# Kernel optimization log

Hardware: AMD Instinct MI355X
Metric: run time of the kernel (lower is better)

## Reference

```python
import jax, jax.numpy as jnp
import numpy as np

NQ, NT, NRF, K, M, B = 8, 16, 4, 4, 2, 28
N_OUTER, N_INNER = 120, 20

def _ry(t):
    c, s = jnp.cos(t / 2), jnp.sin(t / 2)
    return jnp.stack([jnp.stack([c, -s]), jnp.stack([s, c])]).astype(jnp.complex64)

def _rz(t):
    e = jnp.exp(-0.5j * t)
    z = jnp.zeros_like(e)
    return jnp.stack([jnp.stack([e, z]), jnp.stack([z, jnp.conj(e)])])

def _rot(phi, theta, omega):  # pennylane Rot = RZ(omega) RY(theta) RZ(phi)
    return _rz(omega) @ _ry(theta) @ _rz(phi)

def _ap1(state, U, w):
    return jnp.moveaxis(jnp.tensordot(U, state, axes=[[1], [w]]), 0, w)

def _cnot(state, c, t):
    s = jnp.moveaxis(state, (c, t), (0, 1))
    s = s.at[1].set(s[1, ::-1])
    return jnp.moveaxis(s, (0, 1), (c, t))

def _qcircuit(inp, w):  # inp [2*NQ] angles, w [3,NQ,3] -> [NQ] PauliZ expvals
    st = jnp.zeros((2,) * NQ, jnp.complex64).at[(0,) * NQ].set(1.0)
    for i in range(NQ):
        st = _ap1(st, _ry(inp[i]), i)
        st = _ap1(st, _rz(inp[i + NQ]), i)
    for l in range(3):
        for i in range(NQ):
            st = _ap1(st, _rot(w[l, i, 0], w[l, i, 1], w[l, i, 2]), i)
        for i in range(NQ - 1):
            st = _cnot(st, i, i + 1)
        st = _cnot(st, NQ - 1, 0)
    p = jnp.abs(st) ** 2
    z = [jnp.moveaxis(p, i, 0)[0].sum() - jnp.moveaxis(p, i, 0)[1].sum() for i in range(NQ)]
    return jnp.stack(z).astype(jnp.float32)

def _qblock(x, p):  # x [B,80] -> [B,out]
    W1, b1, W2, b2, W3, b3, qw, Wp, bp = p
    h = jnp.tanh(x @ W1.T + b1)
    h = jnp.tanh(h @ W2.T + b2)
    ang = h @ W3.T + b3  # [B, 2*NQ]
    q = jax.vmap(_qcircuit, in_axes=(0, None))(ang, qw)  # [B, NQ]
    return q @ Wp.T + bp

def _to_complex(x):
    return x[..., 0::2] + 1j * x[..., 1::2]

def _sum_rate(H, F, W, Pt):
    Heff = jnp.einsum('kbmn,nbr,kbru->kbmu', H, F[0], W)  # [K,B,M,M]
    G = jnp.einsum('kbmu,kbvu->kbmv', Heff, jnp.conj(Heff))
    A = jnp.eye(M, dtype=G.dtype) + Pt * G
    return jnp.sum(jnp.log2(jnp.abs(jnp.linalg.det(A).real) + 1e-12), axis=0).astype(jnp.float32)

def _beam_err(H, F, W, R, Pt):
    X = jnp.einsum('nbr,kbru->kbnu', F[0], W)  # [K,B,NT,M]
    C = jnp.einsum('kbnu,kbvu->kbnv', X, jnp.conj(X))  # [K,B,NT,NT]
    return jnp.mean(jnp.sqrt(jnp.sum(jnp.abs(C - R) ** 2, axis=(2, 3)) + 1e-12), axis=0).astype(jnp.float32)

def _normalize(F, W, H, Pt):
    F = F / (jnp.abs(F) + 1e-12)
    X = jnp.einsum('nbr,kbru->kbnu', F[0], W)
    pw = jnp.sum(jnp.abs(X) ** 2, axis=(0, 2, 3))  # [B]
    return F, W * jnp.sqrt(Pt / (pw + 1e-12))[None, :, None, None]

def _initialize(H, R, Pt, key):
    k1, k2 = jax.random.split(key)
    ph = jax.random.uniform(k1, (1, NT, B, NRF), maxval=2 * np.pi)
    F = jnp.exp(1j * ph).astype(jnp.complex64)
    W = jax.random.normal(k2, (K, B, NRF, M), dtype=jnp.complex64)
    return _normalize(F, W, H, Pt)

def _state(H, F, W, R, Wproj, bproj):
    s = jnp.concatenate([
        jnp.abs(F).mean((0, 1)).reshape(-1),    # B*NRF
        jnp.angle(F).mean((0, 1)).reshape(-1),  # B*NRF
        jnp.abs(W).mean((0, 1, 2)),             # M
        jnp.angle(W).mean((0, 1, 2)),           # M
        jnp.abs(H).mean((0, 1, 2)).reshape(-1), # NT
        jnp.abs(R).mean((0, 1)).reshape(-1),    # NT*NT  -> total 500
    ])
    return jnp.broadcast_to(s @ Wproj.T + bproj, (B, Wproj.shape[0]))

def _forward(H, R, Pt, step, qFp, qWp, Wproj, bproj):
    F, W = _initialize(H, R, Pt, jax.random.key(1))
    r0, t0 = _sum_rate(H, F, W, Pt), _beam_err(H, F, W, R, Pt)
    base = jax.random.key(7)

    def outer(carry, it):
        F, W = carry
        k = jax.random.fold_in(base, it)
        st = _state(H, F, W, R, Wproj, bproj)  # [B,80]

        def inner(c, p):
            Fc, kk = c
            kk, kn = jax.random.split(kk)
            dF = _to_complex(_qblock(st, p)).reshape(B, NT, NRF).transpose(1, 0, 2)[None]
            noise = jax.random.normal(kn, Fc.shape, dtype=jnp.complex64)
            Fc = Fc + step * noise * 0.001 + dF * 0.001
            return (Fc / (jnp.abs(Fc) + 1e-12), kk), None

        (F, k), _ = jax.lax.scan(inner, (F, k), qFp)
        dW = _to_complex(_qblock(st, qWp)).reshape(B, K, NRF, M).transpose(1, 0, 2, 3)
        k, kn = jax.random.split(k)
        W = W + step * jax.random.normal(kn, W.shape, dtype=jnp.complex64) * 0.001 + dW * 0.001
        F, W = _normalize(F, W, H, Pt)
        return (F, W), (_sum_rate(H, F, W, Pt), _beam_err(H, F, W, R, Pt))

    (F, W), (rs, ts) = jax.lax.scan(outer, (F, W), jnp.arange(N_OUTER))
    rates = jnp.concatenate([r0[None], rs], axis=0).T  # [B, N_OUTER+1]
    taus = jnp.concatenate([t0[None], ts], axis=0).T
    return rates, taus, F, W


def setup_inputs() -> dict:
    key = jax.random.key(0)
    ks = jax.random.split(key, 32)
    r = lambda i, sh: jax.random.normal(ks[i], sh, dtype=jnp.float32)
    WS = 0.1  # weight init scale for tanh stability
    return {
        'H_re': r(0, (K, B, M, NT)), 'H_im': r(1, (K, B, M, NT)),
        'R_re': r(2, (K, B, NT, NT)), 'R_im': r(3, (K, B, NT, NT)),
        'Pt': jnp.ones((1,), jnp.float32),
        'step': jnp.ones((1,), jnp.float32) * 0.02,
        'qF_W1': r(4, (N_INNER, 64, 80)) * WS, 'qF_b1': r(5, (N_INNER, 64)) * WS,
        'qF_W2': r(6, (N_INNER, 32, 64)) * WS, 'qF_b2': r(7, (N_INNER, 32)) * WS,
        'qF_W3': r(8, (N_INNER, 16, 32)) * WS, 'qF_b3': r(9, (N_INNER, 16)) * WS,
        'qF_qw': r(10, (N_INNER, 3, NQ, 3)), 'qF_Wp': r(11, (N_INNER, 128, NQ)) * WS,
        'qF_bp': r(12, (N_INNER, 128)) * WS,
        'qW_W1': r(13, (64, 80)) * WS, 'qW_b1': r(14, (64,)) * WS,
        'qW_W2': r(15, (32, 64)) * WS, 'qW_b2': r(16, (32,)) * WS,
        'qW_W3': r(17, (16, 32)) * WS, 'qW_b3': r(18, (16,)) * WS,
        'qW_qw': r(19, (3, NQ, 3)), 'qW_Wp': r(20, (64, NQ)) * WS,
        'qW_bp': r(21, (64,)) * WS,
        'proj_W': r(22, (80, 500)) * WS, 'proj_b': r(23, (80,)) * WS,
    }


def reference(H_re, H_im, R_re, R_im, Pt, step, qF_W1, qF_b1, qF_W2, qF_b2, qF_W3, qF_b3,
              qF_qw, qF_Wp, qF_bp, qW_W1, qW_b1, qW_W2, qW_b2, qW_W3, qW_b3, qW_qw, qW_Wp,
              qW_bp, proj_W, proj_b):
    H = (H_re + 1j * H_im).astype(jnp.complex64)
    R = (R_re + 1j * R_im).astype(jnp.complex64)
    qFp = (qF_W1, qF_b1, qF_W2, qF_b2, qF_W3, qF_b3, qF_qw, qF_Wp, qF_bp)
    qWp = (qW_W1, qW_b1, qW_W2, qW_b2, qW_W3, qW_b3, qW_qw, qW_Wp, qW_bp)
    return _forward(H, R, Pt[0], step[0], qFp, qWp, proj_W, proj_b)
```

## Files before the change

### kernel.cpp

```cpp
#include <hip/hip_runtime.h>
#include <stdint.h>

#define NT_   16
#define NRF_  4
#define K_    4
#define M_    2
#define B_    28
#define NOUT_ 120
#define NIN_  20
#define FN_   1792
#define WN_   896
#define XN_   3584
#define TJOB_ 8704
#define TSZ_  (21*TJOB_)
#define O_TAUS 3388
#define O_F    6776
#define O_W    10360

typedef float2 cf;
__device__ __forceinline__ cf cmul(cf a, cf b){ return make_float2(a.x*b.x - a.y*b.y, a.x*b.y + a.y*b.x); }
__device__ __forceinline__ cf cmulc(cf a, cf b){ return make_float2(a.x*b.x + a.y*b.y, a.y*b.x - a.x*b.y); }
__device__ __forceinline__ cf cadd(cf a, cf b){ return make_float2(a.x + b.x, a.y + b.y); }
__device__ __forceinline__ cf csc(float s, cf a){ return make_float2(s*a.x, s*a.y); }
__device__ __forceinline__ cf shflc(cf v, int m){ return make_float2(__shfl_xor(v.x, m, 64), __shfl_xor(v.y, m, 64)); }

__device__ __forceinline__ uint32_t rotl32(uint32_t x, int r){ return (x << r) | (x >> (32 - r)); }

__device__ __forceinline__ void threefry(uint32_t k0, uint32_t k1, uint32_t x0, uint32_t x1,
                                         uint32_t &o0, uint32_t &o1){
  uint32_t ks2 = k0 ^ k1 ^ 0x1BD11BDAu;
  x0 += k0; x1 += k1;
#define TF4(a,b,c,d) \
  x0 += x1; x1 = rotl32(x1,(a)); x1 ^= x0; \
  x0 += x1; x1 = rotl32(x1,(b)); x1 ^= x0; \
  x0 += x1; x1 = rotl32(x1,(c)); x1 ^= x0; \
  x0 += x1; x1 = rotl32(x1,(d)); x1 ^= x0;
  TF4(13,15,26,6)  x0 += k1;  x1 += ks2 + 1u;
  TF4(17,29,16,24) x0 += ks2; x1 += k0 + 2u;
  TF4(13,15,26,6)  x0 += k0;  x1 += k1 + 3u;
  TF4(17,29,16,24) x0 += k1;  x1 += ks2 + 4u;
  TF4(13,15,26,6)  x0 += ks2; x1 += k0 + 5u;
#undef TF4
  o0 = x0; o1 = x1;
}

__device__ __forceinline__ void ksplit(uint2 k, uint2 &ka, uint2 &kb){
  threefry(k.x, k.y, 0u, 0u, ka.x, ka.y);
  threefry(k.x, k.y, 0u, 1u, kb.x, kb.y);
}
__device__ __forceinline__ uint2 kfold(uint2 k, uint32_t d){
  uint2 r; threefry(k.x, k.y, 0u, d, r.x, r.y); return r;
}
__device__ __forceinline__ uint32_t rbits(uint2 k, uint32_t i){
  uint32_t a, b; threefry(k.x, k.y, 0u, i, a, b); return a ^ b;
}

__device__ __forceinline__ float bits_to_unit(uint32_t b){
  return __uint_as_float((b >> 9) | 0x3f800000u) - 1.0f;
}

__device__ __forceinline__ float erfinv_f32(float x){
  float w = -log1pf(-x * x);
  float p;
  if (w < 5.0f){
    w = w - 2.5f;
    p =  2.81022636e-08f;
    p = fmaf(p, w,  3.43273939e-07f);
    p = fmaf(p, w, -3.5233877e-06f);
    p = fmaf(p, w, -4.39150654e-06f);
    p = fmaf(p, w,  0.00021858087f);
    p = fmaf(p, w, -0.00125372503f);
    p = fmaf(p, w, -0.00417768164f);
    p = fmaf(p, w,  0.246640727f);
    p = fmaf(p, w,  1.50140941f);
  } else {
    w = sqrtf(w) - 3.0f;
    p = -0.000200214257f;
    p = fmaf(p, w,  0.000100950558f);
    p = fmaf(p, w,  0.00134934322f);
    p = fmaf(p, w, -0.00367342844f);
    p = fmaf(p, w,  0.00573950773f);
    p = fmaf(p, w, -0.0076224613f);
    p = fmaf(p, w,  0.00943887047f);
    p = fmaf(p, w,  1.00167406f);
    p = fmaf(p, w,  2.83297682f);
  }
  return p * x;
}

#define SQRT2F 1.41421356f

__device__ __forceinline__ float normal_from_bits(uint32_t b){
  const float lo = -0.99999994f;
  float u = bits_to_unit(b);
  float v = fmaxf(lo, u * 2.0f + lo);
  return SQRT2F * erfinv_f32(v);
}

__device__ __forceinline__ cf cnormal(uint2 kre, uint2 kim, uint32_t e){
  float re = normal_from_bits(rbits(kre, e));
  float im = normal_from_bits(rbits(kim, e));
  return make_float2(re / SQRT2F, im / SQRT2F);
}

__device__ void noise_key_chain(uint32_t it, uint2 *out){
  uint2 k = kfold(make_uint2(0u, 7u), it);
  for (int j = 0; j < NIN_; ++j){
    uint2 kk, kn;
    ksplit(k, kk, kn);
    k = kk;
    ksplit(kn, out[2*j], out[2*j + 1]);
  }
  uint2 k2, knW;
  ksplit(k, k2, knW);
  ksplit(knW, out[40], out[41]);
}

#define QELEM_ ((NIN_*FN_)/4)
__global__ __launch_bounds__(1024)
void rng_kernel(float2* __restrict__ wsF, float2* __restrict__ wsW,
                float2* __restrict__ wsIW,
                float* __restrict__ wsT, float* __restrict__ wsU,
                float* __restrict__ wsC, float2* __restrict__ wsFst,
                float2* __restrict__ wsWst,
                const float* __restrict__ H_re, const float* __restrict__ H_im,
                const float* __restrict__ R_re, const float* __restrict__ R_im,
                const float* __restrict__ qF_qw, const float* __restrict__ qW_qw,
                const float* __restrict__ qF_W1, const float* __restrict__ qF_W2,
                const float* __restrict__ qF_W3, const float* __restrict__ qF_Wp,
                const float* __restrict__ qW_W1, const float* __restrict__ qW_W2,
                const float* __restrict__ qW_W3, const float* __restrict__ qW_Wp){
  __shared__ uint2 keys[42];
  const int bi = blockIdx.x, t = threadIdx.x;
  if (bi < 4*NOUT_){
    const int it = bi >> 2, q = bi & 3;
    if (t == 0) noise_key_chain((uint32_t)it, keys);
    __syncthreads();
    const int base = q*QELEM_;
    for (int idx = base + t; idx < base + QELEM_; idx += 1024){
      int j = idx / FN_, e = idx - j*FN_;
      wsF[(size_t)it*(NIN_*FN_) + idx] = cnormal(keys[2*j], keys[2*j + 1], (uint32_t)e);
    }
    if (q == 0){
      for (int e = t; e < WN_; e += 1024)
        wsW[(size_t)it*WN_ + e] = cnormal(keys[40], keys[41], (uint32_t)e);
    }
  } else if (bi == 4*NOUT_){
    if (t == 0){
      uint2 k1, k2;
      ksplit(make_uint2(0u, 1u), k1, k2);
      keys[0] = k1;
      ksplit(k2, keys[1], keys[2]);
    }
    __syncthreads();
    const float TWOPI = 6.28318530717958647692f;
    for (int e = t; e < FN_; e += 1024){
      float u = bits_to_unit(rbits(keys[0], (uint32_t)e));
      float ph = fmaxf(0.0f, u * TWOPI);
      float s, c; sincosf(ph, &s, &c);
      wsFst[e] = make_float2(c, s);
    }
    for (int e = t; e < WN_; e += 1024){
      cf w = cnormal(keys[1], keys[2], (uint32_t)e);
      wsIW[e] = w;
      wsWst[e] = w;
    }
  } else if (bi < 4*NOUT_ + 1 + 21){
    const int j = bi - (4*NOUT_ + 1);
    const bool isW = (j == 20);
    const float* W1 = isW ? qW_W1 : qF_W1 + j*(64*80);
    const float* W2 = isW ? qW_W2 : qF_W2 + j*(32*64);
    const float* W3 = isW ? qW_W3 : qF_W3 + j*(16*32);
    const float* Wp = isW ? qW_Wp : qF_Wp + j*(128*8);
    float* dst = wsT + j*TJOB_;
    for (int idx = t; idx < 5120; idx += 1024){
      int q = idx >> 6, i = idx & 63;
      dst[idx] = W1[i*80 + q];
    }
    for (int idx = t; idx < 2048; idx += 1024){
      int q = idx >> 5, i = idx & 31;
      dst[5120 + idx] = W2[i*64 + q];
    }
    for (int idx = t; idx < 512; idx += 1024){
      int q = idx >> 4, i = idx & 15;
      dst[7168 + idx] = W3[i*32 + q];
    }
    const int nOut = isW ? 64 : 128;
    for (int idx = t; idx < 8*nOut; idx += 1024){
      int z = idx / nOut, o = idx - z*nOut;
      dst[7680 + z*128 + o] = Wp[o*8 + z];
    }
  } else {
    if (t < 504){
      int j = t / 24, gg = t - j*24;
      const float* qw = (j == 20) ? qW_qw : qF_qw + j*72;
      float phi = qw[gg*3], th = qw[gg*3 + 1], om = qw[gg*3 + 2];
      float sh, ch; sincosf(0.5f*th, &sh, &ch);
      float sp, cp; sincosf(0.5f*(phi + om), &sp, &cp);
      float sm, cm; sincosf(0.5f*(phi - om), &sm, &cm);
      float* u = wsU + t*8;
      u[0] =  ch*cp; u[1] = -ch*sp;
      u[2] = -sh*cm; u[3] = -sh*sm;
      u[4] =  sh*cm; u[5] = -sh*sm;
      u[6] =  ch*cp; u[7] =  ch*sp;
    } else if (t < 520){
      int n = t - 504;
      float s = 0.f;
      for (int kbm = 0; kbm < 224; ++kbm){
        float re = H_re[kbm*16 + n], im = H_im[kbm*16 + n];
        s += sqrtf(re*re + im*im);
      }
      wsC[n] = s * (1.0f/224.0f);
    } else if (t < 776){
      int nv = t - 520;
      float s = 0.f;
      for (int kb = 0; kb < 112; ++kb){
        float re = R_re[kb*256 + nv], im = R_im[kb*256 + nv];
        s += sqrtf(re*re + im*im);
      }
      wsC[16 + nv] = s * (1.0f/112.0f);
    }
  }
}

__device__ __forceinline__ void gate(int q, cf u00, cf u01, cf u10, cf u11,
                                     cf &a0, cf &a1, cf &a2, cf &a3, int lane){
  if (q == 7){
    cf n0 = cadd(cmul(u00, a0), cmul(u01, a1));
    cf n1 = cadd(cmul(u10, a0), cmul(u11, a1));
    cf n2 = cadd(cmul(u00, a2), cmul(u01, a3));
    cf n3 = cadd(cmul(u10, a2), cmul(u11, a3));
    a0 = n0; a1 = n1; a2 = n2; a3 = n3;
  } else if (q == 6){
    cf n0 = cadd(cmul(u00, a0), cmul(u01, a2));
    cf n2 = cadd(cmul(u10, a0), cmul(u11, a2));
    cf n1 = cadd(cmul(u00, a1), cmul(u01, a3));
    cf n3 = cadd(cmul(u10, a1), cmul(u11, a3));
    a0 = n0; a1 = n1; a2 = n2; a3 = n3;
  } else {
    const int m = 1 << (5 - q);
    const bool hi = (lane & m) != 0;
    cf cO = hi ? u11 : u00;
    cf cP = hi ? u10 : u01;
    cf p0 = shflc(a0, m), p1 = shflc(a1, m), p2 = shflc(a2, m), p3 = shflc(a3, m);
    a0 = cadd(cmul(cO, a0), cmul(cP, p0));
    a1 = cadd(cmul(cO, a1), cmul(cP, p1));
    a2 = cadd(cmul(cO, a2), cmul(cP, p2));
    a3 = cadd(cmul(cO, a3), cmul(cP, p3));
  }
}

__device__ void run_circuit2(const float* trig, const float* uni, int lane, float z[8]){
  cf a0 = make_float2(lane == 0 ? 1.f : 0.f, 0.f);
  cf a1 = make_float2(0.f, 0.f), a2 = make_float2(0.f, 0.f), a3 = make_float2(0.f, 0.f);
  #pragma unroll
  for (int i = 0; i < 8; ++i){
    float sh = trig[2*i],      ch = trig[2*i + 1];
    float sp = trig[16 + 2*i], cp = trig[16 + 2*i + 1];
    float sm = trig[32 + 2*i], cm = trig[32 + 2*i + 1];
    cf u00 = make_float2( ch*cp, -ch*sp);
    cf u11 = make_float2( ch*cp,  ch*sp);
    cf u01 = make_float2(-sh*cm, -sh*sm);
    cf u10 = make_float2( sh*cm, -sh*sm);
    gate(i, u00, u01, u10, u11, a0, a1, a2, a3, lane);
  }
  for (int l = 0; l < 3; ++l){
    #pragma unroll
    for (int i = 0; i < 8; ++i){
      const float* u = uni + (l*8 + i)*8;
      gate(i, make_float2(u[0], u[1]), make_float2(u[2], u[3]),
              make_float2(u[4], u[5]), make_float2(u[6], u[7]), a0, a1, a2, a3, lane);
    }
    #pragma unroll
    for (int i = 0; i < 5; ++i){
      const int cm_ = 1 << (5 - i), tm = 1 << (4 - i);
      const bool c = (lane & cm_) != 0;
      cf p0 = shflc(a0, tm), p1 = shflc(a1, tm), p2 = shflc(a2, tm), p3 = shflc(a3, tm);
      a0 = c ? p0 : a0; a1 = c ? p1 : a1; a2 = c ? p2 : a2; a3 = c ? p3 : a3;
    }
    {
      const bool c = (lane & 1) != 0;
      cf t0 = c ? a2 : a0, t2 = c ? a0 : a2;
      cf t1 = c ? a3 : a1, t3 = c ? a1 : a3;
      a0 = t0; a1 = t1; a2 = t2; a3 = t3;
    }
    { cf tmp = a2; a2 = a3; a3 = tmp; }
    a1 = shflc(a1, 32);
    a3 = shflc(a3, 32);
  }
  const float p0 = a0.x*a0.x + a0.y*a0.y;
  const float p1 = a1.x*a1.x + a1.y*a1.y;
  const float p2 = a2.x*a2.x + a2.y*a2.y;
  const float p3 = a3.x*a3.x + a3.y*a3.y;
  const float tot = p0 + p1 + p2 + p3;
  z[6] = (p0 + p1) - (p2 + p3);
  z[7] = (p0 + p2) - (p1 + p3);
  #pragma unroll
  for (int i = 0; i < 6; ++i)
    z[i] = ((lane >> (5 - i)) & 1) ? -tot : tot;
  #pragma unroll
  for (int m = 1; m < 64; m <<= 1){
    #pragma unroll
    for (int i = 0; i < 8; ++i) z[i] += __shfl_xor(z[i], m, 64);
  }
}

__global__ __launch_bounds__(640)
void k_qblock2(const float* __restrict__ wsT, const float* __restrict__ wsU,
               const float* __restrict__ wsC,
               const float* __restrict__ wsFeatA, const float* __restrict__ wsFeatG,
               const float* __restrict__ wsPart,
               const float* __restrict__ projW, const float* __restrict__ projB,
               const float* __restrict__ qF_b1, const float* __restrict__ qF_b2,
               const float* __restrict__ qF_b3, const float* __restrict__ qF_bp,
               const float* __restrict__ qW_b1, const float* __restrict__ qW_b2,
               const float* __restrict__ qW_b3, const float* __restrict__ qW_bp,
               float2* __restrict__ wsdF, float2* __restrict__ wsdW){
  const int j = blockIdx.x;
  const int t = threadIdx.x;
  const int lane = t & 63;
  const int wv = t >> 6;
  const bool isW = (j == 20);
  __shared__ float sS[500];
  __shared__ float sSt[80];
  __shared__ float mlp[160];
  __shared__ float luni[192];
  for (int i = t; i < 192; i += 640) luni[i] = wsU[j*192 + i];
  for (int i = t; i < 112; i += 640){ sS[i] = wsFeatA[i]; sS[112 + i] = wsFeatG[i]; }
  if (t < 4){
    float s = 0.f;
    for (int bb = 0; bb < 28; ++bb) s += wsPart[bb*4 + t];
    sS[224 + t] = s * (1.0f/448.0f);
  }
  for (int i = t; i < 272; i += 640) sS[228 + i] = wsC[i];
  __syncthreads();
  {
    int o = wv*8 + (lane >> 3), i = lane & 7;
    const float* row = projW + o*500;
    float acc = 0.f;
    #pragma unroll
    for (int s = 0; s < 63; ++s){
      int j2 = i + 8*s;
      if (j2 < 500) acc = fmaf(sS[j2], row[j2], acc);
    }
    #pragma unroll
    for (int m = 1; m < 8; m <<= 1) acc += __shfl_xor(acc, m, 64);
    if (i == 0) sSt[o] = acc + projB[o];
  }
  __syncthreads();

  if (t < 64){
    const float* b1 = isW ? qW_b1 : qF_b1 + j*64;
    const float* b2 = isW ? qW_b2 : qF_b2 + j*32;
    const float* b3 = isW ? qW_b3 : qF_b3 + j*16;
    const float* bp = isW ? qW_bp : qF_bp + j*128;
    const float* w1t = wsT + j*TJOB_;
    const float* w2t = w1t + 5120;
    const float* w3t = w1t + 7168;
    const float* wpt = w1t + 7680;

    {
      float acc = b1[lane];
      for (int q = 0; q < 80; ++q) acc = fmaf(w1t[q*64 + lane], sSt[q], acc);
      mlp[lane] = tanhf(acc);
    }
    __builtin_amdgcn_wave_barrier();
    {
      int i2 = lane & 31;
      float acc = b2[i2];
      for (int q = 0; q < 64; ++q) acc = fmaf(w2t[q*32 + i2], mlp[q], acc);
      float h2 = tanhf(acc);
      __builtin_amdgcn_wave_barrier();
      if (lane < 32) mlp[64 + lane] = h2;
    }
    __builtin_amdgcn_wave_barrier();
    {
      int i3 = lane & 15;
      float acc = b3[i3];
      for (int q = 0; q < 32; ++q) acc = fmaf(w3t[q*16 + i3], mlp[64 + q], acc);
      __builtin_amdgcn_wave_barrier();
      if (lane < 16) mlp[96 + lane] = acc;
    }
    __builtin_amdgcn_wave_barrier();
    if (lane < 24){
      int i = lane & 7, which = lane >> 3;
      float th = mlp[96 + i], om = mlp[96 + 8 + i];
      float arg = (which == 0) ? 0.5f*th
                : (which == 1) ? 0.5f*(0.f + om)
                               : 0.5f*(0.f - om);
      float s, c; sincosf(arg, &s, &c);
      mlp[112 + which*16 + 2*i]     = s;
      mlp[112 + which*16 + 2*i + 1] = c;
    }
    __builtin_amdgcn_wave_barrier();
    float z[8];
    run_circuit2(mlp + 112, luni, lane, z);
    if (!isW){
      float o0 = bp[lane];
      float o1 = bp[64 + lane];
      #pragma unroll
      for (int i = 0; i < 8; ++i){
        o0 = fmaf(wpt[i*128 + lane],      z[i], o0);
        o1 = fmaf(wpt[i*128 + 64 + lane], z[i], o1);
      }
      __builtin_amdgcn_wave_barrier();
      mlp[lane] = o0; mlp[64 + lane] = o1;
      __builtin_amdgcn_wave_barrier();
      wsdF[j*64 + lane] = make_float2(mlp[2*lane], mlp[2*lane + 1]);
    } else {
      float o0 = bp[lane];
      #pragma unroll
      for (int i = 0; i < 8; ++i) o0 = fmaf(wpt[i*128 + lane], z[i], o0);
      __builtin_amdgcn_wave_barrier();
      mlp[lane] = o0;
      __builtin_amdgcn_wave_barrier();
      if (lane < 32) wsdW[lane] = make_float2(mlp[2*lane], mlp[2*lane + 1]);
    }
  }
}

__global__ __launch_bounds__(128)
void k_update(const float* __restrict__ H_re, const float* __restrict__ H_im,
              const float* __restrict__ R_re, const float* __restrict__ R_im,
              const float* __restrict__ Pt_p, const float* __restrict__ step_p,
              const float2* __restrict__ wsF, const float2* __restrict__ wsW,
              const float2* __restrict__ wsdF, const float2* __restrict__ wsdW,
              float2* __restrict__ wsFst, float2* __restrict__ wsWst,
              float* __restrict__ wsFeatA, float* __restrict__ wsFeatG,
              float* __restrict__ wsPart,
              float* __restrict__ out, int it, int mode){
  const int b = blockIdx.x;
  const int t = threadIdx.x;
  __shared__ cf lF[64];
  __shared__ cf lW[32];
  __shared__ cf lX[128];
  __shared__ float scrA[96], scrG[96];
  __shared__ float red2[2];
  __shared__ float sscale;
  __shared__ float heR[16], heI[16];
  __shared__ float sKBl[4], sKB2l[4];
  const float c1 = step_p[0] * 0.001f;
  const float Ptv = Pt_p[0];

  if (t < 64){
    const int n = t >> 2, r = t & 3;
    const int e = n*112 + b*4 + r;
    cf F = wsFst[e];
    if (mode){
      const float2* np = wsF + (size_t)it*(NIN_*FN_);
      cf nzA[10], dvA[10], nzB[10], dvB[10];
      #pragma unroll
      for (int s = 0; s < 10; ++s){ nzA[s] = np[s*FN_ + e];        dvA[s] = wsdF[s*64 + t]; }
      #pragma unroll
      for (int s = 0; s < 10; ++s){ nzB[s] = np[(10 + s)*FN_ + e]; dvB[s] = wsdF[(10 + s)*64 + t]; }
      #pragma unroll
      for (int s = 0; s < 10; ++s){
        F.x = F.x + c1*nzA[s].x + 0.001f*dvA[s].x;
        F.y = F.y + c1*nzA[s].y + 0.001f*dvA[s].y;
        float rr = sqrtf(F.x*F.x + F.y*F.y) + 1e-12f;
        F.x /= rr; F.y /= rr;
      }
      #pragma unroll
      for (int s = 0; s < 10; ++s){
        F.x = F.x + c1*nzB[s].x + 0.001f*dvB[s].x;
        F.y = F.y + c1*nzB[s].y + 0.001f*dvB[s].y;
        float rr = sqrtf(F.x*F.x + F.y*F.y) + 1e-12f;
        F.x /= rr; F.y /= rr;
      }
    }
    float rr = sqrtf(F.x*F.x + F.y*F.y) + 1e-12f;
    F.x /= rr; F.y /= rr;
    lF[t] = F;
    wsFst[e] = F;
  } else if (t < 96){
    const int wi = t - 64;
    const int k = wi >> 3, ru = wi & 7;
    const int ew = (k*28 + b)*8 + ru;
    cf w = wsWst[ew];
    if (mode){
      cf nw = wsW[(size_t)it*WN_ + ew];
      cf dw = wsdW[k*8 + ru];
      w.x = w.x + c1*nw.x + 0.001f*dw.x;
      w.y = w.y + c1*nw.y + 0.001f*dw.y;
    }
    lW[wi] = w;
  }
  __syncthreads();
  {
    int u = t & 1, n = (t >> 1) & 15, k = t >> 5;
    const cf* fr = lF + n*4;
    const cf* wr = lW + k*8 + u;
    cf acc = cmul(fr[0], wr[0]);
    acc = cadd(acc, cmul(fr[1], wr[2]));
    acc = cadd(acc, cmul(fr[2], wr[4]));
    acc = cadd(acc, cmul(fr[3], wr[6]));
    lX[t] = acc;
  }
  __syncthreads();
  {
    float s = lX[t].x*lX[t].x + lX[t].y*lX[t].y;
    #pragma unroll
    for (int m = 1; m < 64; m <<= 1) s += __shfl_xor(s, m, 64);
    if ((t & 63) == 0) red2[t >> 6] = s;
  }
  __syncthreads();
  if (t == 0) sscale = sqrtf(Ptv / ((red2[0] + red2[1]) + 1e-12f));
  __syncthreads();
  const float sc = sscale;
  if (t < 32){
    const int k = t >> 3, ru = t & 7;
    const int ew = (k*28 + b)*8 + ru;
    cf w = csc(sc, lW[t]);
    lW[t] = w;
    wsWst[ew] = w;
  }
  lX[t] = csc(sc, lX[t]);
  __syncthreads();
  if (t < 16){
    const int k = t >> 2, ent = t & 3;
    const int m = ent >> 1, u = ent & 1;
    const float* hr = H_re + (k*28 + b)*32 + m*16;
    const float* hi = H_im + (k*28 + b)*32 + m*16;
    cf He = make_float2(0.f, 0.f);
    for (int n = 0; n < 16; ++n){
      cf h = make_float2(hr[n], hi[n]);
      He = cadd(He, cmul(h, lX[k*32 + n*2 + u]));
    }
    heR[t] = He.x; heI[t] = He.y;
  }
  __builtin_amdgcn_wave_barrier();
  if (t < 4){
    const int k = t;
    cf He00 = make_float2(heR[k*4 + 0], heI[k*4 + 0]);
    cf He01 = make_float2(heR[k*4 + 1], heI[k*4 + 1]);
    cf He10 = make_float2(heR[k*4 + 2], heI[k*4 + 2]);
    cf He11 = make_float2(heR[k*4 + 3], heI[k*4 + 3]);
    cf G00 = cadd(cmulc(He00, He00), cmulc(He01, He01));
    cf G01 = cadd(cmulc(He00, He10), cmulc(He01, He11));
    cf G10 = cadd(cmulc(He10, He00), cmulc(He11, He01));
    cf G11 = cadd(cmulc(He10, He10), cmulc(He11, He11));
    cf A00 = make_float2(1.f + Ptv*G00.x, Ptv*G00.y);
    cf A01 = csc(Ptv, G01);
    cf A10 = csc(Ptv, G10);
    cf A11 = make_float2(1.f + Ptv*G11.x, Ptv*G11.y);
    float detre = (A00.x*A11.x - A00.y*A11.y) - (A01.x*A10.x - A01.y*A10.y);
    sKBl[k] = log2f(fabsf(detre) + 1e-12f);
  }
  {
    const int k = t >> 5, i = t & 31;
    const float* rr = R_re + (k*28 + b)*256;
    const float* ri = R_im + (k*28 + b)*256;
    float acc = 0.f;
    #pragma unroll
    for (int c = 0; c < 8; ++c){
      int nv = c*32 + i;
      int n = nv >> 4, v = nv & 15;
      cf xn0 = lX[k*32 + n*2], xn1 = lX[k*32 + n*2 + 1];
      cf xv0 = lX[k*32 + v*2], xv1 = lX[k*32 + v*2 + 1];
      cf C = cadd(cmulc(xn0, xv0), cmulc(xn1, xv1));
      float dr = C.x - rr[nv], di = C.y - ri[nv];
      acc += dr*dr + di*di;
    }
    #pragma unroll
    for (int m = 1; m < 32; m <<= 1) acc += __shfl_xor(acc, m, 64);
    if (i == 0) sKB2l[k] = sqrtf(acc + 1e-12f);
  }
  __syncthreads();
  if (t == 0){
    const int slot = mode ? (it + 1) : 0;
    out[b*121 + slot] = sKBl[0] + sKBl[1] + sKBl[2] + sKBl[3];
    out[O_TAUS + b*121 + slot] = 0.25f*(sKB2l[0] + sKB2l[1] + sKB2l[2] + sKB2l[3]);
  }
  if (t < 64){
    cf f = lF[t];
    scrA[t] = sqrtf(f.x*f.x + f.y*f.y);
    scrG[t] = atan2f(f.y, f.x);
  } else if (t < 96){
    cf w = lW[t - 64];
    scrA[t] = sqrtf(w.x*w.x + w.y*w.y);
    scrG[t] = atan2f(w.y, w.x);
  }
  __syncthreads();
  if (t < 8){
    int r = t & 3;
    const float* src = (t < 4) ? scrA : scrG;
    float s = 0.f;
    for (int n = 0; n < 16; ++n) s += src[n*4 + r];
    float* dst = (t < 4) ? wsFeatA : wsFeatG;
    dst[b*4 + r] = s * (1.0f/16.0f);
  } else if (t >= 8 && t < 12){
    int tt = t - 8;
    int u = tt & 1; bool isG = tt >= 2;
    const float* src = isG ? scrG : scrA;
    float s = 0.f;
    for (int i = 0; i < 16; ++i) s += src[64 + i*2 + u];
    wsPart[b*4 + tt] = s;
  }
}

__global__ __launch_bounds__(1024)
void k_out(const float2* __restrict__ wsFst, const float2* __restrict__ wsWst,
           float* __restrict__ out, int fmode){
  const int t = threadIdx.x;
  if (fmode == 1){
    for (int e = t; e < FN_; e += 1024){
      out[O_F + e]       = wsFst[e].x;
      out[O_F + FN_ + e] = wsFst[e].y;
    }
    for (int e = t; e < WN_; e += 1024){
      out[O_W + e]       = wsWst[e].x;
      out[O_W + WN_ + e] = wsWst[e].y;
    }
  } else if (fmode == 2){
    for (int e = t; e < FN_; e += 1024) out[O_F + e] = wsFst[e].x;
    for (int e = t; e < WN_; e += 1024) out[O_F + FN_ + e] = wsWst[e].x;
  } else {
    for (int e = t; e < FN_; e += 1024){
      out[O_F + 2*e]     = wsFst[e].x;
      out[O_F + 2*e + 1] = wsFst[e].y;
    }
    for (int e = t; e < WN_; e += 1024){
      out[O_W + 2*e]     = wsWst[e].x;
      out[O_W + 2*e + 1] = wsWst[e].y;
    }
  }
}

__global__ __launch_bounds__(1024)
void main_kernel(const float* __restrict__ H_re, const float* __restrict__ H_im,
                 const float* __restrict__ R_re, const float* __restrict__ R_im,
                 const float* __restrict__ Pt_p, const float* __restrict__ step_p,
                 const float* __restrict__ qF_W1, const float* __restrict__ qF_b1,
                 const float* __restrict__ qF_W2, const float* __restrict__ qF_b2,
                 const float* __restrict__ qF_W3, const float* __restrict__ qF_b3,
                 const float* __restrict__ qF_qw, const float* __restrict__ qF_Wp,
                 const float* __restrict__ qF_bp,
                 const float* __restrict__ qW_W1, const float* __restrict__ qW_b1,
                 const float* __restrict__ qW_W2, const float* __restrict__ qW_b2,
                 const float* __restrict__ qW_W3, const float* __restrict__ qW_b3,
                 const float* __restrict__ qW_qw, const float* __restrict__ qW_Wp,
                 const float* __restrict__ qW_bp,
                 const float* __restrict__ projW, const float* __restrict__ projB,
                 float* __restrict__ out, int fmode)
{
  const int t = threadIdx.x;
  const int lane = t & 63;
  const int wv = t >> 6;

  __shared__ cf sF[FN_];
  __shared__ cf sW[WN_];
  __shared__ float sS[500];
  __shared__ float sSt[80];
  __shared__ float sScale[B_];
  __shared__ float sKB[112];
  __shared__ float sKB2[112];
  __shared__ float sRed[64];
  __shared__ uint2 sKeys[42];
  __shared__ float sPar[2];
  __shared__ float sUni[21*24*8];
  __shared__ __align__(16) unsigned char uPool[XN_ * sizeof(cf)];
  cf*    sX   = (cf*)uPool;
  cf*    sdF  = (cf*)uPool;
  cf*    sdW  = (cf*)(uPool + NIN_*64*sizeof(cf));
  float* sMLP = (float*)(uPool + NIN_*64*sizeof(cf) + 32*sizeof(cf));

  if (t == 0){ sPar[0] = step_p[0]; sPar[1] = Pt_p[0]; }

  if (t < 504){
    int j = t / 24, gg = t - j*24;
    const float* qw = (j == 20) ? qW_qw : qF_qw + j*72;
    float phi = qw[gg*3], th = qw[gg*3 + 1], om = qw[gg*3 + 2];
    float sh, ch; sincosf(0.5f*th, &sh, &ch);
    float sp, cp; sincosf(0.5f*(phi + om), &sp, &cp);
    float sm, cm; sincosf(0.5f*(phi - om), &sm, &cm);
    float* u = sUni + t*8;
    u[0] =  ch*cp; u[1] = -ch*sp;
    u[2] = -sh*cm; u[3] = -sh*sm;
    u[4] =  sh*cm; u[5] = -sh*sm;
    u[6] =  ch*cp; u[7] =  ch*sp;
  }

  {
    float* scratch = (float*)uPool;
    float local = 0.f;
    for (int i = t; i < 3584; i += 1024) local += sqrtf(H_re[i]*H_re[i] + H_im[i]*H_im[i]);
    scratch[t] = local;
    __syncthreads();
    for (int s = 512; s >= 16; s >>= 1){
      if (t < s) scratch[t] += scratch[t + s];
      __syncthreads();
    }
    if (t < 16) sS[228 + t] = scratch[t] * (1.0f/224.0f);
    __syncthreads();
    local = 0.f;
    for (int i = t; i < 28672; i += 1024) local += sqrtf(R_re[i]*R_re[i] + R_im[i]*R_im[i]);
    scratch[t] = local;
    __syncthreads();
    for (int s = 512; s >= 256; s >>= 1){
      if (t < s) scratch[t] += scratch[t + s];
      __syncthreads();
    }
    if (t < 256) sS[244 + t] = scratch[t] * (1.0f/112.0f);
    __syncthreads();
  }

  {
    if (t == 0){
      uint2 k1, k2; ksplit(make_uint2(0u, 1u), k1, k2);
      sKeys[0] = k1; ksplit(k2, sKeys[1], sKeys[2]);
    }
    __syncthreads();
    const float TWOPI = 6.28318530717958647692f;
    for (int e = t; e < FN_; e += 1024){
      float u = bits_to_unit(rbits(sKeys[0], (uint32_t)e));
      float ph = fmaxf(0.0f, u * TWOPI);
      float s, c; sincosf(ph, &s, &c);
      sF[e] = make_float2(c, s);
    }
    for (int e = t; e < WN_; e += 1024) sW[e] = cnormal(sKeys[1], sKeys[2], (uint32_t)e);
  }
  __syncthreads();

  const float stepv = sPar[0], Ptv = sPar[1];
  const float c1 = stepv * 0.001f;

  for (int it = -1; it < NOUT_; ++it){
    if (it >= 0){
      if (t == 0) noise_key_chain((uint32_t)it, sKeys);
      __syncthreads();
      if (t < 112){
        float sa = 0.f, sg = 0.f;
        for (int n = 0; n < NT_; ++n){
          cf f = sF[n*112 + t];
          sa += sqrtf(f.x*f.x + f.y*f.y);
          sg += atan2f(f.y, f.x);
        }
        sS[t]       = sa * (1.0f/16.0f);
        sS[112 + t] = sg * (1.0f/16.0f);
      }
      {
        float aW = 0.f, gW = 0.f;
        if (t < WN_){
          cf w = sW[t];
          aW = sqrtf(w.x*w.x + w.y*w.y);
          gW = atan2f(w.y, w.x);
        }
        #pragma unroll
        for (int m = 2; m < 64; m <<= 1){
          aW += __shfl_xor(aW, m, 64);
          gW += __shfl_xor(gW, m, 64);
        }
        if (t < WN_ && lane < 2){
          sRed[wv*2 + lane] = aW;
          sRed[32 + wv*2 + lane] = gW;
        }
      }
      __syncthreads();
      if (t < 4){
        int u = t & 1;
        int base = (t >= 2) ? 32 : 0;
        float s = 0.f;
        for (int w = 0; w < 14; ++w) s += sRed[base + w*2 + u];
        sS[224 + t] = s * (1.0f/448.0f);
      }
      __syncthreads();
      if (t < 640){
        int o = t >> 3, i = t & 7;
        const float* row = projW + o*500;
        float acc = 0.f;
        for (int j = i; j < 500; j += 8) acc = fmaf(sS[j], row[j], acc);
        #pragma unroll
        for (int m = 1; m < 8; m <<= 1) acc += __shfl_xor(acc, m, 64);
        if (i == 0) sSt[o] = acc + projB[o];
      }
      __syncthreads();
      for (int rnd = 0; rnd < 2; ++rnd){
        int j = wv + rnd*16;
        if (j < 21){
          const bool isW = (j == 20);
          const float* b1 = isW ? qW_b1 : qF_b1 + j*64;
          const float* b2 = isW ? qW_b2 : qF_b2 + j*32;
          const float* b3 = isW ? qW_b3 : qF_b3 + j*16;
          const float* bp = isW ? qW_bp : qF_bp + j*128;
          float* mlp = sMLP + wv*160;
          const float* W1 = isW ? qW_W1 : qF_W1 + j*(64*80);
          const float* W2 = isW ? qW_W2 : qF_W2 + j*(32*64);
          const float* W3 = isW ? qW_W3 : qF_W3 + j*(16*32);
          const float* Wp = isW ? qW_Wp : qF_Wp + j*(128*8);
          {
            const float* row = W1 + lane*80;
            float acc = b1[lane];
            for (int q = 0; q < 80; ++q) acc = fmaf(row[q], sSt[q], acc);
            mlp[lane] = tanhf(acc);
          }
          __builtin_amdgcn_wave_barrier();
          {
            int i2 = lane & 31;
            const float* row = W2 + i2*64;
            float acc = b2[i2];
            for (int q = 0; q < 64; ++q) acc = fmaf(row[q], mlp[q], acc);
            float h2 = tanhf(acc);
            __builtin_amdgcn_wave_barrier();
            if (lane < 32) mlp[64 + lane] = h2;
          }
          __builtin_amdgcn_wave_barrier();
          {
            int i3 = lane & 15;
            const float* row = W3 + i3*32;
            float acc = b3[i3];
            for (int q = 0; q < 32; ++q) acc = fmaf(row[q], mlp[64 + q], acc);
            __builtin_amdgcn_wave_barrier();
            if (lane < 16) mlp[96 + lane] = acc;
          }
          __builtin_amdgcn_wave_barrier();
          if (lane < 24){
            int i = lane & 7, which = lane >> 3;
            float th = mlp[96 + i], om = mlp[96 + 8 + i];
            float arg = (which == 0) ? 0.5f*th
                      : (which == 1) ? 0.5f*(0.f + om)
                                     : 0.5f*(0.f - om);
            float s, c; sincosf(arg, &s, &c);
            mlp[112 + which*16 + 2*i]     = s;
            mlp[112 + which*16 + 2*i + 1] = c;
          }
          __builtin_amdgcn_wave_barrier();
          float z[8];
          run_circuit2(mlp + 112, sUni + j*192, lane, z);
          if (!isW){
            float o0 = bp[lane];
            float o1 = bp[64 + lane];
            const float* r0 = Wp + lane*8;
            const float* r1 = Wp + (64 + lane)*8;
            #pragma unroll
            for (int i = 0; i < 8; ++i){
              o0 = fmaf(r0[i], z[i], o0);
              o1 = fmaf(r1[i], z[i], o1);
            }
            __builtin_amdgcn_wave_barrier();
            mlp[lane] = o0; mlp[64 + lane] = o1;
            __builtin_amdgcn_wave_barrier();
            sdF[j*64 + lane] = make_float2(mlp[2*lane], mlp[2*lane + 1]);
          } else {
            float o0 = bp[lane];
            const float* r0 = Wp + lane*8;
            #pragma unroll
            for (int i = 0; i < 8; ++i) o0 = fmaf(r0[i], z[i], o0);
            __builtin_amdgcn_wave_barrier();
            mlp[lane] = o0;
            __builtin_amdgcn_wave_barrier();
            if (lane < 32) sdW[lane] = make_float2(mlp[2*lane], mlp[2*lane + 1]);
          }
        }
      }
      __syncthreads();
      if (t < 896){
        cf f0 = sF[t], f1 = sF[t + 896];
        const int dfi0 = (t/112)*4 + (t & 3);
        const int dfi1 = dfi0 + 32;
        for (int j = 0; j < NIN_; ++j){
          cf n0 = cnormal(sKeys[2*j], sKeys[2*j + 1], (uint32_t)t);
          cf n1 = cnormal(sKeys[2*j], sKeys[2*j + 1], (uint32_t)(t + 896));
          cf d0 = sdF[j*64 + dfi0], d1 = sdF[j*64 + dfi1];
          f0.x = f0.x + c1*n0.x + 0.001f*d0.x;
          f0.y = f0.y + c1*n0.y + 0.001f*d0.y;
          f1.x = f1.x + c1*n1.x + 0.001f*d1.x;
          f1.y = f1.y + c1*n1.y + 0.001f*d1.y;
          float r0 = sqrtf(f0.x*f0.x + f0.y*f0.y) + 1e-12f;
          float r1 = sqrtf(f1.x*f1.x + f1.y*f1.y) + 1e-12f;
          f0.x /= r0; f0.y /= r0;
          f1.x /= r1; f1.y /= r1;
        }
        sF[t] = f0; sF[t + 896] = f1;
      }
      if (t < 448){
        cf w0 = sW[t], w1 = sW[t + 448];
        cf n0 = cnormal(sKeys[40], sKeys[41], (uint32_t)t);
        cf n1 = cnormal(sKeys[40], sKeys[41], (uint32_t)(t + 448));
        int dwi0 = (t/224)*8 + (t & 7);
        int dwi1 = ((t + 448)/224)*8 + (t & 7);
        cf d0 = sdW[dwi0], d1 = sdW[dwi1];
        w0.x = w0.x + c1*n0.x + 0.001f*d0.x;
        w0.y = w0.y + c1*n0.y + 0.001f*d0.y;
        w1.x = w1.x + c1*n1.x + 0.001f*d1.x;
        w1.y = w1.y + c1*n1.y + 0.001f*d1.y;
        sW[t] = w0; sW[t + 448] = w1;
      }
      __syncthreads();
    }

    for (int e = t; e < FN_; e += 1024){
      cf f = sF[e];
      float r = sqrtf(f.x*f.x + f.y*f.y) + 1e-12f;
      f.x /= r; f.y /= r;
      sF[e] = f;
    }
    __syncthreads();
    for (int x = t; x < XN_; x += 1024){
      int u = x & 1, n = (x >> 1) & 15, kb = x >> 5;
      int b = kb - (kb/28)*28;
      const cf* fr = sF + n*112 + b*4;
      const cf* wr = sW + kb*8 + u;
      cf acc = cmul(fr[0], wr[0]);
      acc = cadd(acc, cmul(fr[1], wr[2]));
      acc = cadd(acc, cmul(fr[2], wr[4]));
      acc = cadd(acc, cmul(fr[3], wr[6]));
      sX[x] = acc;
    }
    __syncthreads();
    if (t < 896){
      int b = t >> 5, i = t & 31;
      float s = 0.f;
      #pragma unroll
      for (int k = 0; k < 4; ++k){
        cf v = sX[(k*28 + b)*32 + i];
        s += v.x*v.x + v.y*v.y;
      }
      #pragma unroll
      for (int m = 1; m < 32; m <<= 1) s += __shfl_xor(s, m, 64);
      if (i == 0) sScale[b] = sqrtf(Ptv / (s + 1e-12f));
    }
    __syncthreads();
    for (int e = t; e < WN_; e += 1024){
      int kb = e >> 3;
      sW[e] = csc(sScale[kb - (kb/28)*28], sW[e]);
    }
    for (int x = t; x < XN_; x += 1024){
      int kb = x >> 5;
      sX[x] = csc(sScale[kb - (kb/28)*28], sX[x]);
    }
    __syncthreads();
    if (t < 112){
      const int kb = t;
      cf He00 = make_float2(0.f,0.f), He01 = He00, He10 = He00, He11 = He00;
      const float* hr = H_re + kb*32;
      const float* hi = H_im + kb*32;
      for (int n = 0; n < 16; ++n){
        cf x0 = sX[kb*32 + n*2], x1 = sX[kb*32 + n*2 + 1];
        cf h0 = make_float2(hr[n],      hi[n]);
        cf h1 = make_float2(hr[16 + n], hi[16 + n]);
        He00 = cadd(He00, cmul(h0, x0));
        He01 = cadd(He01, cmul(h0, x1));
        He10 = cadd(He10, cmul(h1, x0));
        He11 = cadd(He11, cmul(h1, x1));
      }
      cf G00 = cadd(cmulc(He00, He00), cmulc(He01, He01));
      cf G01 = cadd(cmulc(He00, He10), cmulc(He01, He11));
      cf G10 = cadd(cmulc(He10, He00), cmulc(He11, He01));
      cf G11 = cadd(cmulc(He10, He10), cmulc(He11, He11));
      cf A00 = make_float2(1.f + Ptv*G00.x, Ptv*G00.y);
      cf A01 = csc(Ptv, G01);
      cf A10 = csc(Ptv, G10);
      cf A11 = make_float2(1.f + Ptv*G11.x, Ptv*G11.y);
      float detre = (A00.x*A11.x - A00.y*A11.y) - (A01.x*A10.x - A01.y*A10.y);
      sKB[kb] = log2f(fabsf(detre) + 1e-12f);
    }
    if (t >= 128){
      int tt = t - 128, kb = tt >> 3, i = tt & 7;
      const float* rr = R_re + kb*256;
      const float* ri = R_im + kb*256;
      float acc = 0.f;
      for (int c = 0; c < 32; ++c){
        int nv = i + (c << 3);
        int n = nv >> 4, v = nv & 15;
        cf xn0 = sX[kb*32 + n*2], xn1 = sX[kb*32 + n*2 + 1];
        cf xv0 = sX[kb*32 + v*2], xv1 = sX[kb*32 + v*2 + 1];
        cf C = cadd(cmulc(xn0, xv0), cmulc(xn1, xv1));
        float dr = C.x - rr[nv], di = C.y - ri[nv];
        acc += dr*dr + di*di;
      }
      #pragma unroll
      for (int m = 1; m < 8; m <<= 1) acc += __shfl_xor(acc, m, 64);
      if (i == 0) sKB2[kb] = sqrtf(acc + 1e-12f);
    }
    __syncthreads();
    if (t < 28){
      const int slot = it + 1;
      out[t*121 + slot] = sKB[t] + sKB[28 + t] + sKB[56 + t] + sKB[84 + t];
      out[O_TAUS + t*121 + slot] = 0.25f*(sKB2[t] + sKB2[28 + t] + sKB2[56 + t] + sKB2[84 + t]);
    }
    __syncthreads();
  }

  if (fmode == 1){
    for (int e = t; e < FN_; e += 1024){
      out[O_F + e]       = sF[e].x;
      out[O_F + FN_ + e] = sF[e].y;
    }
    for (int e = t; e < WN_; e += 1024){
      out[O_W + e]       = sW[e].x;
      out[O_W + WN_ + e] = sW[e].y;
    }
  } else if (fmode == 2){
    for (int e = t; e < FN_; e += 1024) out[O_F + e] = sF[e].x;
    for (int e = t; e < WN_; e += 1024) out[O_F + FN_ + e] = sW[e].x;
  } else {
    for (int e = t; e < FN_; e += 1024){
      out[O_F + 2*e]     = sF[e].x;
      out[O_F + 2*e + 1] = sF[e].y;
    }
    for (int e = t; e < WN_; e += 1024){
      out[O_W + 2*e]     = sW[e].x;
      out[O_W + 2*e + 1] = sW[e].y;
    }
  }
}

extern "C" void kernel_launch(void* const* d_in, const int* in_sizes, int n_in,
                              void* d_out, int out_size, void* d_ws, size_t ws_size,
                              hipStream_t stream){
  (void)in_sizes; (void)n_in;
  const float* H_re  = (const float*)d_in[0];
  const float* H_im  = (const float*)d_in[1];
  const float* R_re  = (const float*)d_in[2];
  const float* R_im  = (const float*)d_in[3];
  const float* Pt    = (const float*)d_in[4];
  const float* stp   = (const float*)d_in[5];
  const float* qF_W1 = (const float*)d_in[6];
  const float* qF_b1 = (const float*)d_in[7];
  const float* qF_W2 = (const float*)d_in[8];
  const float* qF_b2 = (const float*)d_in[9];
  const float* qF_W3 = (const float*)d_in[10];
  const float* qF_b3 = (const float*)d_in[11];
  const float* qF_qw = (const float*)d_in[12];
  const float* qF_Wp = (const float*)d_in[13];
  const float* qF_bp = (const float*)d_in[14];
  const float* qW_W1 = (const float*)d_in[15];
  const float* qW_b1 = (const float*)d_in[16];
  const float* qW_W2 = (const float*)d_in[17];
  const float* qW_b2 = (const float*)d_in[18];
  const float* qW_W3 = (const float*)d_in[19];
  const float* qW_b3 = (const float*)d_in[20];
  const float* qW_qw = (const float*)d_in[21];
  const float* qW_Wp = (const float*)d_in[22];
  const float* qW_bp = (const float*)d_in[23];
  const float* projW = (const float*)d_in[24];
  const float* projB = (const float*)d_in[25];
  float* out = (float*)d_out;

  int fmode = 0;
  if (out_size == 12152) fmode = 1;
  else if (out_size == 9464) fmode = 2;

  const size_t nF = (size_t)NOUT_ * NIN_ * FN_;
  const size_t nW = (size_t)NOUT_ * WN_;
  const size_t need = (nF + nW + WN_ + FN_ + WN_ + 1280 + 32) * sizeof(float2)
                    + (TSZ_ + 4032 + 272 + 112 + 112 + 112 + 4) * sizeof(float);
  const int useWs = (d_ws != nullptr && ws_size >= need) ? 1 : 0;

  float2* wsF  = (float2*)d_ws;
  float2* wsW  = wsF + nF;
  float2* wsIW = wsW + nW;
  float*  wsT  = (float*)(wsIW + WN_);
  float*  wsU  = wsT + TSZ_;
  float*  wsC  = wsU + 4032;
  float2* wsFst = (float2*)(wsC + 272);
  float2* wsWst = wsFst + FN_;
  float2* wsdF  = wsWst + WN_;
  float2* wsdW  = wsdF + 1280;
  float*  wsFeatA = (float*)(wsdW + 32);
  float*  wsFeatG = wsFeatA + 112;
  float*  wsPart  = wsFeatG + 112;

  if (useWs){
    rng_kernel<<<dim3(4*NOUT_ + 1 + 21 + 1), dim3(1024), 0, stream>>>(
        wsF, wsW, wsIW, wsT, wsU, wsC, wsFst, wsWst,
        H_re, H_im, R_re, R_im, qF_qw, qW_qw,
        qF_W1, qF_W2, qF_W3, qF_Wp, qW_W1, qW_W2, qW_W3, qW_Wp);
    k_update<<<dim3(B_), dim3(128), 0, stream>>>(
        H_re, H_im, R_re, R_im, Pt, stp, wsF, wsW, wsdF, wsdW,
        wsFst, wsWst, wsFeatA, wsFeatG, wsPart, out, 0, 0);
    for (int it = 0; it < NOUT_; ++it){
      k_qblock2<<<dim3(21), dim3(640), 0, stream>>>(
          wsT, wsU, wsC, wsFeatA, wsFeatG, wsPart, projW, projB,
          qF_b1, qF_b2, qF_b3, qF_bp, qW_b1, qW_b2, qW_b3, qW_bp,
          wsdF, wsdW);
      k_update<<<dim3(B_), dim3(128), 0, stream>>>(
          H_re, H_im, R_re, R_im, Pt, stp, wsF, wsW, wsdF, wsdW,
          wsFst, wsWst, wsFeatA, wsFeatG, wsPart, out, it, 1);
    }
    k_out<<<dim3(1), dim3(1024), 0, stream>>>(wsFst, wsWst, out, fmode);
  } else {
    main_kernel<<<dim3(1), dim3(1024), 0, stream>>>(
        H_re, H_im, R_re, R_im, Pt, stp,
        qF_W1, qF_b1, qF_W2, qF_b2, qF_W3, qF_b3, qF_qw, qF_Wp, qF_bp,
        qW_W1, qW_b1, qW_W2, qW_b2, qW_W3, qW_b3, qW_qw, qW_Wp, qW_bp,
        projW, projB, out, fmode);
  }
}
```

Measured before the change: 2.493 ms.

## Fuse per-iteration qblock and update kernels with atomic flag handoff

Merges the quantum-block kernel and the per-batch update kernel into one 49-workgroup launch per outer iteration. The 21 qblock workgroups signal completion through an agent-scope atomic counter, and the 28 update workgroups prefetch their noise and state values before spinning on that flag. Feature buffers are double-buffered across iterations so the update blocks can write next-iteration features while the qblock blocks read the current ones. This halves the number of kernel launches and overlaps the update blocks' global loads with qblock compute. In exchange it relies on all 49 workgroups being co-resident, and the fallback path without workspace no longer runs the main kernel.

```diff
diff --git a/kernel.cpp b/kernel.cpp
--- a/kernel.cpp
+++ b/kernel.cpp
@@ -306,131 +306,34 @@
 }
 
 __global__ __launch_bounds__(640)
-void k_qblock2(const float* __restrict__ wsT, const float* __restrict__ wsU,
-               const float* __restrict__ wsC,
-               const float* __restrict__ wsFeatA, const float* __restrict__ wsFeatG,
-               const float* __restrict__ wsPart,
-               const float* __restrict__ projW, const float* __restrict__ projB,
-               const float* __restrict__ qF_b1, const float* __restrict__ qF_b2,
-               const float* __restrict__ qF_b3, const float* __restrict__ qF_bp,
-               const float* __restrict__ qW_b1, const float* __restrict__ qW_b2,
-               const float* __restrict__ qW_b3, const float* __restrict__ qW_bp,
-               float2* __restrict__ wsdF, float2* __restrict__ wsdW){
-  const int j = blockIdx.x;
+void k_iter(const float* __restrict__ H_re, const float* __restrict__ H_im,
+            const float* __restrict__ R_re, const float* __restrict__ R_im,
+            const float* __restrict__ Pt_p, const float* __restrict__ step_p,
+            const float* __restrict__ wsT, const float* __restrict__ wsU,
+            const float* __restrict__ wsC,
+            const float* __restrict__ featInA, const float* __restrict__ featInG,
+            const float* __restrict__ featInP,
+            float* __restrict__ featOutA, float* __restrict__ featOutG,
+            float* __restrict__ featOutP,
+            const float* __restrict__ projW, const float* __restrict__ projB,
+            const float* __restrict__ qF_b1, const float* __restrict__ qF_b2,
+            const float* __restrict__ qF_b3, const float* __restrict__ qF_bp,
+            const float* __restrict__ qW_b1, const float* __restrict__ qW_b2,
+            const float* __restrict__ qW_b3, const float* __restrict__ qW_bp,
+            const float2* __restrict__ wsF, const float2* __restrict__ wsW,
+            float2* __restrict__ wsdF, float2* __restrict__ wsdW,
+            float2* __restrict__ wsFst, float2* __restrict__ wsWst,
+            uint32_t* __restrict__ flag, uint32_t target,
+            float* __restrict__ out, int it)
+{
+  const int wg = blockIdx.x;
   const int t = threadIdx.x;
   const int lane = t & 63;
   const int wv = t >> 6;
-  const bool isW = (j == 20);
   __shared__ float sS[500];
   __shared__ float sSt[80];
   __shared__ float mlp[160];
   __shared__ float luni[192];
-  for (int i = t; i < 192; i += 640) luni[i] = wsU[j*192 + i];
-  for (int i = t; i < 112; i += 640){ sS[i] = wsFeatA[i]; sS[112 + i] = wsFeatG[i]; }
-  if (t < 4){
-    float s = 0.f;
-    for (int bb = 0; bb < 28; ++bb) s += wsPart[bb*4 + t];
-    sS[224 + t] = s * (1.0f/448.0f);
-  }
-  for (int i = t; i < 272; i += 640) sS[228 + i] = wsC[i];
-  __syncthreads();
-  {
-    int o = wv*8 + (lane >> 3), i = lane & 7;
-    const float* row = projW + o*500;
-    float acc = 0.f;
-    #pragma unroll
-    for (int s = 0; s < 63; ++s){
-      int j2 = i + 8*s;
-      if (j2 < 500) acc = fmaf(sS[j2], row[j2], acc);
-    }
-    #pragma unroll
-    for (int m = 1; m < 8; m <<= 1) acc += __shfl_xor(acc, m, 64);
-    if (i == 0) sSt[o] = acc + projB[o];
-  }
-  __syncthreads();
-
-  if (t < 64){
-    const float* b1 = isW ? qW_b1 : qF_b1 + j*64;
-    const float* b2 = isW ? qW_b2 : qF_b2 + j*32;
-    const float* b3 = isW ? qW_b3 : qF_b3 + j*16;
-    const float* bp = isW ? qW_bp : qF_bp + j*128;
-    const float* w1t = wsT + j*TJOB_;
-    const float* w2t = w1t + 5120;
-    const float* w3t = w1t + 7168;
-    const float* wpt = w1t + 7680;
-
-    {
-      float acc = b1[lane];
-      for (int q = 0; q < 80; ++q) acc = fmaf(w1t[q*64 + lane], sSt[q], acc);
-      mlp[lane] = tanhf(acc);
-    }
-    __builtin_amdgcn_wave_barrier();
-    {
-      int i2 = lane & 31;
-      float acc = b2[i2];
-      for (int q = 0; q < 64; ++q) acc = fmaf(w2t[q*32 + i2], mlp[q], acc);
-      float h2 = tanhf(acc);
-      __builtin_amdgcn_wave_barrier();
-      if (lane < 32) mlp[64 + lane] = h2;
-    }
-    __builtin_amdgcn_wave_barrier();
-    {
-      int i3 = lane & 15;
-      float acc = b3[i3];
-      for (int q = 0; q < 32; ++q) acc = fmaf(w3t[q*16 + i3], mlp[64 + q], acc);
-      __builtin_amdgcn_wave_barrier();
-      if (lane < 16) mlp[96 + lane] = acc;
-    }
-    __builtin_amdgcn_wave_barrier();
-    if (lane < 24){
-      int i = lane & 7, which = lane >> 3;
-      float th = mlp[96 + i], om = mlp[96 + 8 + i];
-      float arg = (which == 0) ? 0.5f*th
-                : (which == 1) ? 0.5f*(0.f + om)
-                               : 0.5f*(0.f - om);
-      float s, c; sincosf(arg, &s, &c);
-      mlp[112 + which*16 + 2*i]     = s;
-      mlp[112 + which*16 + 2*i + 1] = c;
-    }
-    __builtin_amdgcn_wave_barrier();
-    float z[8];
-    run_circuit2(mlp + 112, luni, lane, z);
-    if (!isW){
-      float o0 = bp[lane];
-      float o1 = bp[64 + lane];
-      #pragma unroll
-      for (int i = 0; i < 8; ++i){
-        o0 = fmaf(wpt[i*128 + lane],      z[i], o0);
-        o1 = fmaf(wpt[i*128 + 64 + lane], z[i], o1);
-      }
-      __builtin_amdgcn_wave_barrier();
-      mlp[lane] = o0; mlp[64 + lane] = o1;
-      __builtin_amdgcn_wave_barrier();
-      wsdF[j*64 + lane] = make_float2(mlp[2*lane], mlp[2*lane + 1]);
-    } else {
-      float o0 = bp[lane];
-      #pragma unroll
-      for (int i = 0; i < 8; ++i) o0 = fmaf(wpt[i*128 + lane], z[i], o0);
-      __builtin_amdgcn_wave_barrier();
-      mlp[lane] = o0;
-      __builtin_amdgcn_wave_barrier();
-      if (lane < 32) wsdW[lane] = make_float2(mlp[2*lane], mlp[2*lane + 1]);
-    }
-  }
-}
-
-__global__ __launch_bounds__(128)
-void k_update(const float* __restrict__ H_re, const float* __restrict__ H_im,
-              const float* __restrict__ R_re, const float* __restrict__ R_im,
-              const float* __restrict__ Pt_p, const float* __restrict__ step_p,
-              const float2* __restrict__ wsF, const float2* __restrict__ wsW,
-              const float2* __restrict__ wsdF, const float2* __restrict__ wsdW,
-              float2* __restrict__ wsFst, float2* __restrict__ wsWst,
-              float* __restrict__ wsFeatA, float* __restrict__ wsFeatG,
-              float* __restrict__ wsPart,
-              float* __restrict__ out, int it, int mode){
-  const int b = blockIdx.x;
-  const int t = threadIdx.x;
   __shared__ cf lF[64];
   __shared__ cf lW[32];
   __shared__ cf lX[128];
@@ -439,54 +342,173 @@
   __shared__ float sscale;
   __shared__ float heR[16], heI[16];
   __shared__ float sKBl[4], sKB2l[4];
+
+  if (wg < 21){
+    const int j = wg;
+    const bool isW = (j == 20);
+    for (int i = t; i < 192; i += 640) luni[i] = wsU[j*192 + i];
+    for (int i = t; i < 112; i += 640){ sS[i] = featInA[i]; sS[112 + i] = featInG[i]; }
+    if (t < 4){
+      float s = 0.f;
+      for (int bb = 0; bb < 28; ++bb) s += featInP[bb*4 + t];
+      sS[224 + t] = s * (1.0f/448.0f);
+    }
+    for (int i = t; i < 272; i += 640) sS[228 + i] = wsC[i];
+    __syncthreads();
+    {
+      int o = wv*8 + (lane >> 3), i = lane & 7;
+      const float* row = projW + o*500;
+      float acc = 0.f;
+      #pragma unroll
+      for (int s = 0; s < 63; ++s){
+        int j2 = i + 8*s;
+        if (j2 < 500) acc = fmaf(sS[j2], row[j2], acc);
+      }
+      #pragma unroll
+      for (int m = 1; m < 8; m <<= 1) acc += __shfl_xor(acc, m, 64);
+      if (i == 0) sSt[o] = acc + projB[o];
+    }
+    __syncthreads();
+    if (t < 64){
+      const float* b1 = isW ? qW_b1 : qF_b1 + j*64;
+      const float* b2 = isW ? qW_b2 : qF_b2 + j*32;
+      const float* b3 = isW ? qW_b3 : qF_b3 + j*16;
+      const float* bp = isW ? qW_bp : qF_bp + j*128;
+      const float* w1t = wsT + j*TJOB_;
+      const float* w2t = w1t + 5120;
+      const float* w3t = w1t + 7168;
+      const float* wpt = w1t + 7680;
+      {
+        float acc = b1[lane];
+        for (int q = 0; q < 80; ++q) acc = fmaf(w1t[q*64 + lane], sSt[q], acc);
+        mlp[lane] = tanhf(acc);
+      }
+      __builtin_amdgcn_wave_barrier();
+      {
+        int i2 = lane & 31;
+        float acc = b2[i2];
+        for (int q = 0; q < 64; ++q) acc = fmaf(w2t[q*32 + i2], mlp[q], acc);
+        float h2 = tanhf(acc);
+        __builtin_amdgcn_wave_barrier();
+        if (lane < 32) mlp[64 + lane] = h2;
+      }
+      __builtin_amdgcn_wave_barrier();
+      {
+        int i3 = lane & 15;
+        float acc = b3[i3];
+        for (int q = 0; q < 32; ++q) acc = fmaf(w3t[q*16 + i3], mlp[64 + q], acc);
+        __builtin_amdgcn_wave_barrier();
+        if (lane < 16) mlp[96 + lane] = acc;
+      }
+      __builtin_amdgcn_wave_barrier();
+      if (lane < 24){
+        int i = lane & 7, which = lane >> 3;
+        float th = mlp[96 + i], om = mlp[96 + 8 + i];
+        float arg = (which == 0) ? 0.5f*th
+                  : (which == 1) ? 0.5f*(0.f + om)
+                                 : 0.5f*(0.f - om);
+        float s, c; sincosf(arg, &s, &c);
+        mlp[112 + which*16 + 2*i]     = s;
+        mlp[112 + which*16 + 2*i + 1] = c;
+      }
+      __builtin_amdgcn_wave_barrier();
+      float z[8];
+      run_circuit2(mlp + 112, luni, lane, z);
+      if (!isW){
+        float o0 = bp[lane];
+        float o1 = bp[64 + lane];
+        #pragma unroll
+        for (int i = 0; i < 8; ++i){
+          o0 = fmaf(wpt[i*128 + lane],      z[i], o0);
+          o1 = fmaf(wpt[i*128 + 64 + lane], z[i], o1);
+        }
+        __builtin_amdgcn_wave_barrier();
+        mlp[lane] = o0; mlp[64 + lane] = o1;
+        __builtin_amdgcn_wave_barrier();
+        wsdF[j*64 + lane] = make_float2(mlp[2*lane], mlp[2*lane + 1]);
+      } else {
+        float o0 = bp[lane];
+        #pragma unroll
+        for (int i = 0; i < 8; ++i) o0 = fmaf(wpt[i*128 + lane], z[i], o0);
+        __builtin_amdgcn_wave_barrier();
+        mlp[lane] = o0;
+        __builtin_amdgcn_wave_barrier();
+        if (lane < 32) wsdW[lane] = make_float2(mlp[2*lane], mlp[2*lane + 1]);
+      }
+    }
+    __syncthreads();
+    if (t == 0){
+      __threadfence();
+      __hip_atomic_fetch_add(flag, 1u, __ATOMIC_RELAXED, __HIP_MEMORY_SCOPE_AGENT);
+    }
+    return;
+  }
+
+  const int b = wg - 21;
   const float c1 = step_p[0] * 0.001f;
   const float Ptv = Pt_p[0];
 
+  cf F;
+  cf nzA[10], nzB[10];
+  cf w, nw;
   if (t < 64){
     const int n = t >> 2, r = t & 3;
     const int e = n*112 + b*4 + r;
-    cf F = wsFst[e];
-    if (mode){
-      const float2* np = wsF + (size_t)it*(NIN_*FN_);
-      cf nzA[10], dvA[10], nzB[10], dvB[10];
-      #pragma unroll
-      for (int s = 0; s < 10; ++s){ nzA[s] = np[s*FN_ + e];        dvA[s] = wsdF[s*64 + t]; }
-      #pragma unroll
-      for (int s = 0; s < 10; ++s){ nzB[s] = np[(10 + s)*FN_ + e]; dvB[s] = wsdF[(10 + s)*64 + t]; }
-      #pragma unroll
-      for (int s = 0; s < 10; ++s){
-        F.x = F.x + c1*nzA[s].x + 0.001f*dvA[s].x;
-        F.y = F.y + c1*nzA[s].y + 0.001f*dvA[s].y;
-        float rr = sqrtf(F.x*F.x + F.y*F.y) + 1e-12f;
-        F.x /= rr; F.y /= rr;
-      }
-      #pragma unroll
-      for (int s = 0; s < 10; ++s){
-        F.x = F.x + c1*nzB[s].x + 0.001f*dvB[s].x;
-        F.y = F.y + c1*nzB[s].y + 0.001f*dvB[s].y;
-        float rr = sqrtf(F.x*F.x + F.y*F.y) + 1e-12f;
-        F.x /= rr; F.y /= rr;
-      }
+    F = wsFst[e];
+    const float2* np = wsF + (size_t)it*(NIN_*FN_);
+    #pragma unroll
+    for (int s = 0; s < 10; ++s) nzA[s] = np[s*FN_ + e];
+    #pragma unroll
+    for (int s = 0; s < 10; ++s) nzB[s] = np[(10 + s)*FN_ + e];
+  } else if (t < 96){
+    const int wi = t - 64;
+    const int k = wi >> 3, ru = wi & 7;
+    const int ew = (k*28 + b)*8 + ru;
+    w  = wsWst[ew];
+    nw = wsW[(size_t)it*WN_ + ew];
+  }
+  if (t == 0){
+    while (__hip_atomic_load(flag, __ATOMIC_RELAXED, __HIP_MEMORY_SCOPE_AGENT) < target)
+      __builtin_amdgcn_s_sleep(1);
+    __threadfence();
+  }
+  __syncthreads();
+
+  if (t < 64){
+    cf dvA[10], dvB[10];
+    #pragma unroll
+    for (int s = 0; s < 10; ++s) dvA[s] = wsdF[s*64 + t];
+    #pragma unroll
+    for (int s = 0; s < 10; ++s) dvB[s] = wsdF[(10 + s)*64 + t];
+    #pragma unroll
+    for (int s = 0; s < 10; ++s){
+      F.x = F.x + c1*nzA[s].x + 0.001f*dvA[s].x;
+      F.y = F.y + c1*nzA[s].y + 0.001f*dvA[s].y;
+      float rr = sqrtf(F.x*F.x + F.y*F.y) + 1e-12f;
+      F.x /= rr; F.y /= rr;
+    }
+    #pragma unroll
+    for (int s = 0; s < 10; ++s){
+      F.x = F.x + c1*nzB[s].x + 0.001f*dvB[s].x;
+      F.y = F.y + c1*nzB[s].y + 0.001f*dvB[s].y;
+      float rr = sqrtf(F.x*F.x + F.y*F.y) + 1e-12f;
+      F.x /= rr; F.y /= rr;
     }
     float rr = sqrtf(F.x*F.x + F.y*F.y) + 1e-12f;
     F.x /= rr; F.y /= rr;
     lF[t] = F;
+    const int e = (t >> 2)*112 + b*4 + (t & 3);
     wsFst[e] = F;
   } else if (t < 96){
     const int wi = t - 64;
     const int k = wi >> 3, ru = wi & 7;
-    const int ew = (k*28 + b)*8 + ru;
-    cf w = wsWst[ew];
-    if (mode){
-      cf nw = wsW[(size_t)it*WN_ + ew];
-      cf dw = wsdW[k*8 + ru];
-      w.x = w.x + c1*nw.x + 0.001f*dw.x;
-      w.y = w.y + c1*nw.y + 0.001f*dw.y;
-    }
+    cf dw = wsdW[k*8 + ru];
+    w.x = w.x + c1*nw.x + 0.001f*dw.x;
+    w.y = w.y + c1*nw.y + 0.001f*dw.y;
     lW[wi] = w;
   }
   __syncthreads();
-  {
+  if (t < 128){
     int u = t & 1, n = (t >> 1) & 15, k = t >> 5;
     const cf* fr = lF + n*4;
     const cf* wr = lW + k*8 + u;
@@ -497,7 +519,7 @@
     lX[t] = acc;
   }
   __syncthreads();
-  {
+  if (t < 128){
     float s = lX[t].x*lX[t].x + lX[t].y*lX[t].y;
     #pragma unroll
     for (int m = 1; m < 64; m <<= 1) s += __shfl_xor(s, m, 64);
@@ -510,11 +532,11 @@
   if (t < 32){
     const int k = t >> 3, ru = t & 7;
     const int ew = (k*28 + b)*8 + ru;
-    cf w = csc(sc, lW[t]);
-    lW[t] = w;
-    wsWst[ew] = w;
-  }
-  lX[t] = csc(sc, lX[t]);
+    cf ww = csc(sc, lW[t]);
+    lW[t] = ww;
+    wsWst[ew] = ww;
+  }
+  if (t < 128) lX[t] = csc(sc, lX[t]);
   __syncthreads();
   if (t < 16){
     const int k = t >> 2, ent = t & 3;
@@ -546,7 +568,7 @@
     float detre = (A00.x*A11.x - A00.y*A11.y) - (A01.x*A10.x - A01.y*A10.y);
     sKBl[k] = log2f(fabsf(detre) + 1e-12f);
   }
-  {
+  if (t < 128){
     const int k = t >> 5, i = t & 31;
     const float* rr = R_re + (k*28 + b)*256;
     const float* ri = R_im + (k*28 + b)*256;
@@ -567,9 +589,155 @@
   }
   __syncthreads();
   if (t == 0){
-    const int slot = mode ? (it + 1) : 0;
+    const int slot = it + 1;
     out[b*121 + slot] = sKBl[0] + sKBl[1] + sKBl[2] + sKBl[3];
     out[O_TAUS + b*121 + slot] = 0.25f*(sKB2l[0] + sKB2l[1] + sKB2l[2] + sKB2l[3]);
+  }
+  if (t < 64){
+    cf f = lF[t];
+    scrA[t] = sqrtf(f.x*f.x + f.y*f.y);
+    scrG[t] = atan2f(f.y, f.x);
+  } else if (t < 96){
+    cf ww = lW[t - 64];
+    scrA[t] = sqrtf(ww.x*ww.x + ww.y*ww.y);
+    scrG[t] = atan2f(ww.y, ww.x);
+  }
+  __syncthreads();
+  if (t < 8){
+    int r = t & 3;
+    const float* src = (t < 4) ? scrA : scrG;
+    float s = 0.f;
+    for (int n = 0; n < 16; ++n) s += src[n*4 + r];
+    float* dst = (t < 4) ? featOutA : featOutG;
+    dst[b*4 + r] = s * (1.0f/16.0f);
+  } else if (t >= 8 && t < 12){
+    int tt = t - 8;
+    int u = tt & 1; bool isG = tt >= 2;
+    const float* src = isG ? scrG : scrA;
+    float s = 0.f;
+    for (int i = 0; i < 16; ++i) s += src[64 + i*2 + u];
+    featOutP[b*4 + tt] = s;
+  }
+}
+
+__global__ __launch_bounds__(128)
+void k_update(const float* __restrict__ H_re, const float* __restrict__ H_im,
+              const float* __restrict__ R_re, const float* __restrict__ R_im,
+              const float* __restrict__ Pt_p, const float* __restrict__ step_p,
+              float2* __restrict__ wsFst, float2* __restrict__ wsWst,
+              float* __restrict__ wsFeatA, float* __restrict__ wsFeatG,
+              float* __restrict__ wsPart,
+              float* __restrict__ out){
+  const int b = blockIdx.x;
+  const int t = threadIdx.x;
+  __shared__ cf lF[64];
+  __shared__ cf lW[32];
+  __shared__ cf lX[128];
+  __shared__ float scrA[96], scrG[96];
+  __shared__ float red2[2];
+  __shared__ float sscale;
+  __shared__ float heR[16], heI[16];
+  __shared__ float sKBl[4], sKB2l[4];
+  const float Ptv = Pt_p[0];
+  (void)step_p;
+
+  if (t < 64){
+    const int n = t >> 2, r = t & 3;
+    const int e = n*112 + b*4 + r;
+    cf F = wsFst[e];
+    float rr = sqrtf(F.x*F.x + F.y*F.y) + 1e-12f;
+    F.x /= rr; F.y /= rr;
+    lF[t] = F;
+    wsFst[e] = F;
+  } else if (t < 96){
+    const int wi = t - 64;
+    const int k = wi >> 3, ru = wi & 7;
+    lW[wi] = wsWst[(k*28 + b)*8 + ru];
+  }
+  __syncthreads();
+  {
+    int u = t & 1, n = (t >> 1) & 15, k = t >> 5;
+    const cf* fr = lF + n*4;
+    const cf* wr = lW + k*8 + u;
+    cf acc = cmul(fr[0], wr[0]);
+    acc = cadd(acc, cmul(fr[1], wr[2]));
+    acc = cadd(acc, cmul(fr[2], wr[4]));
+    acc = cadd(acc, cmul(fr[3], wr[6]));
+    lX[t] = acc;
+  }
+  __syncthreads();
+  {
+    float s = lX[t].x*lX[t].x + lX[t].y*lX[t].y;
+    #pragma unroll
+    for (int m = 1; m < 64; m <<= 1) s += __shfl_xor(s, m, 64);
+    if ((t & 63) == 0) red2[t >> 6] = s;
+  }
+  __syncthreads();
+  if (t == 0) sscale = sqrtf(Ptv / ((red2[0] + red2[1]) + 1e-12f));
+  __syncthreads();
+  const float sc = sscale;
+  if (t < 32){
+    const int k = t >> 3, ru = t & 7;
+    const int ew = (k*28 + b)*8 + ru;
+    cf w = csc(sc, lW[t]);
+    lW[t] = w;
+    wsWst[ew] = w;
+  }
+  lX[t] = csc(sc, lX[t]);
+  __syncthreads();
+  if (t < 16){
+    const int k = t >> 2, ent = t & 3;
+    const int m = ent >> 1, u = ent & 1;
+    const float* hr = H_re + (k*28 + b)*32 + m*16;
+    const float* hi = H_im + (k*28 + b)*32 + m*16;
+    cf He = make_float2(0.f, 0.f);
+    for (int n = 0; n < 16; ++n){
+      cf h = make_float2(hr[n], hi[n]);
+      He = cadd(He, cmul(h, lX[k*32 + n*2 + u]));
+    }
+    heR[t] = He.x; heI[t] = He.y;
+  }
+  __builtin_amdgcn_wave_barrier();
+  if (t < 4){
+    const int k = t;
+    cf He00 = make_float2(heR[k*4 + 0], heI[k*4 + 0]);
+    cf He01 = make_float2(heR[k*4 + 1], heI[k*4 + 1]);
+    cf He10 = make_float2(heR[k*4 + 2], heI[k*4 + 2]);
+    cf He11 = make_float2(heR[k*4 + 3], heI[k*4 + 3]);
+    cf G00 = cadd(cmulc(He00, He00), cmulc(He01, He01));
+    cf G01 = cadd(cmulc(He00, He10), cmulc(He01, He11));
+    cf G10 = cadd(cmulc(He10, He00), cmulc(He11, He01));
+    cf G11 = cadd(cmulc(He10, He10), cmulc(He11, He11));
+    cf A00 = make_float2(1.f + Ptv*G00.x, Ptv*G00.y);
+    cf A01 = csc(Ptv, G01);
+    cf A10 = csc(Ptv, G10);
+    cf A11 = make_float2(1.f + Ptv*G11.x, Ptv*G11.y);
+    float detre = (A00.x*A11.x - A00.y*A11.y) - (A01.x*A10.x - A01.y*A10.y);
+    sKBl[k] = log2f(fabsf(detre) + 1e-12f);
+  }
+  {
+    const int k = t >> 5, i = t & 31;
+    const float* rr = R_re + (k*28 + b)*256;
+    const float* ri = R_im + (k*28 + b)*256;
+    float acc = 0.f;
+    #pragma unroll
+    for (int c = 0; c < 8; ++c){
+      int nv = c*32 + i;
+      int n = nv >> 4, v = nv & 15;
+      cf xn0 = lX[k*32 + n*2], xn1 = lX[k*32 + n*2 + 1];
+      cf xv0 = lX[k*32 + v*2], xv1 = lX[k*32 + v*2 + 1];
+      cf C = cadd(cmulc(xn0, xv0), cmulc(xn1, xv1));
+      float dr = C.x - rr[nv], di = C.y - ri[nv];
+      acc += dr*dr + di*di;
+    }
+    #pragma unroll
+    for (int m = 1; m < 32; m <<= 1) acc += __shfl_xor(acc, m, 64);
+    if (i == 0) sKB2l[k] = sqrtf(acc + 1e-12f);
+  }
+  __syncthreads();
+  if (t == 0){
+    out[b*121 + 0] = sKBl[0] + sKBl[1] + sKBl[2] + sKBl[3];
+    out[O_TAUS + b*121 + 0] = 0.25f*(sKB2l[0] + sKB2l[1] + sKB2l[2] + sKB2l[3]);
   }
   if (t < 64){
     cf f = lF[t];
@@ -622,385 +790,6 @@
     for (int e = t; e < WN_; e += 1024){
       out[O_W + 2*e]     = wsWst[e].x;
       out[O_W + 2*e + 1] = wsWst[e].y;
-    }
-  }
-}
-
-__global__ __launch_bounds__(1024)
-void main_kernel(const float* __restrict__ H_re, const float* __restrict__ H_im,
-                 const float* __restrict__ R_re, const float* __restrict__ R_im,
-                 const float* __restrict__ Pt_p, const float* __restrict__ step_p,
-                 const float* __restrict__ qF_W1, const float* __restrict__ qF_b1,
-                 const float* __restrict__ qF_W2, const float* __restrict__ qF_b2,
-                 const float* __restrict__ qF_W3, const float* __restrict__ qF_b3,
-                 const float* __restrict__ qF_qw, const float* __restrict__ qF_Wp,
-                 const float* __restrict__ qF_bp,
-                 const float* __restrict__ qW_W1, const float* __restrict__ qW_b1,
-                 const float* __restrict__ qW_W2, const float* __restrict__ qW_b2,
-                 const float* __restrict__ qW_W3, const float* __restrict__ qW_b3,
-                 const float* __restrict__ qW_qw, const float* __restrict__ qW_Wp,
-                 const float* __restrict__ qW_bp,
-                 const float* __restrict__ projW, const float* __restrict__ projB,
-                 float* __restrict__ out, int fmode)
-{
-  const int t = threadIdx.x;
-  const int lane = t & 63;
-  const int wv = t >> 6;
-
-  __shared__ cf sF[FN_];
-  __shared__ cf sW[WN_];
-  __shared__ float sS[500];
-  __shared__ float sSt[80];
-  __shared__ float sScale[B_];
-  __shared__ float sKB[112];
-  __shared__ float sKB2[112];
-  __shared__ float sRed[64];
-  __shared__ uint2 sKeys[42];
-  __shared__ float sPar[2];
-  __shared__ float sUni[21*24*8];
-  __shared__ __align__(16) unsigned char uPool[XN_ * sizeof(cf)];
-  cf*    sX   = (cf*)uPool;
-  cf*    sdF  = (cf*)uPool;
-  cf*    sdW  = (cf*)(uPool + NIN_*64*sizeof(cf));
-  float* sMLP = (float*)(uPool + NIN_*64*sizeof(cf) + 32*sizeof(cf));
-
-  if (t == 0){ sPar[0] = step_p[0]; sPar[1] = Pt_p[0]; }
-
-  if (t < 504){
-    int j = t / 24, gg = t - j*24;
-    const float* qw = (j == 20) ? qW_qw : qF_qw + j*72;
-    float phi = qw[gg*3], th = qw[gg*3 + 1], om = qw[gg*3 + 2];
-    float sh, ch; sincosf(0.5f*th, &sh, &ch);
-    float sp, cp; sincosf(0.5f*(phi + om), &sp, &cp);
-    float sm, cm; sincosf(0.5f*(phi - om), &sm, &cm);
-    float* u = sUni + t*8;
-    u[0] =  ch*cp; u[1] = -ch*sp;
-    u[2] = -sh*cm; u[3] = -sh*sm;
-    u[4] =  sh*cm; u[5] = -sh*sm;
-    u[6] =  ch*cp; u[7] =  ch*sp;
-  }
-
-  {
-    float* scratch = (float*)uPool;
-    float local = 0.f;
-    for (int i = t; i < 3584; i += 1024) local += sqrtf(H_re[i]*H_re[i] + H_im[i]*H_im[i]);
-    scratch[t] = local;
-    __syncthreads();
-    for (int s = 512; s >= 16; s >>= 1){
-      if (t < s) scratch[t] += scratch[t + s];
-      __syncthreads();
-    }
-    if (t < 16) sS[228 + t] = scratch[t] * (1.0f/224.0f);
-    __syncthreads();
-    local = 0.f;
-    for (int i = t; i < 28672; i += 1024) local += sqrtf(R_re[i]*R_re[i] + R_im[i]*R_im[i]);
-    scratch[t] = local;
-    __syncthreads();
-    for (int s = 512; s >= 256; s >>= 1){
-      if (t < s) scratch[t] += scratch[t + s];
-      __syncthreads();
-    }
-    if (t < 256) sS[244 + t] = scratch[t] * (1.0f/112.0f);
-    __syncthreads();
-  }
-
-  {
-    if (t == 0){
-      uint2 k1, k2; ksplit(make_uint2(0u, 1u), k1, k2);
-      sKeys[0] = k1; ksplit(k2, sKeys[1], sKeys[2]);
-    }
-    __syncthreads();
-    const float TWOPI = 6.28318530717958647692f;
-    for (int e = t; e < FN_; e += 1024){
-      float u = bits_to_unit(rbits(sKeys[0], (uint32_t)e));
-      float ph = fmaxf(0.0f, u * TWOPI);
-      float s, c; sincosf(ph, &s, &c);
-      sF[e] = make_float2(c, s);
-    }
-    for (int e = t; e < WN_; e += 1024) sW[e] = cnormal(sKeys[1], sKeys[2], (uint32_t)e);
-  }
-  __syncthreads();
-
-  const float stepv = sPar[0], Ptv = sPar[1];
-  const float c1 = stepv * 0.001f;
-
-  for (int it = -1; it < NOUT_; ++it){
-    if (it >= 0){
-      if (t == 0) noise_key_chain((uint32_t)it, sKeys);
-      __syncthreads();
-      if (t < 112){
-        float sa = 0.f, sg = 0.f;
-        for (int n = 0; n < NT_; ++n){
-          cf f = sF[n*112 + t];
-          sa += sqrtf(f.x*f.x + f.y*f.y);
-          sg += atan2f(f.y, f.x);
-        }
-        sS[t]       = sa * (1.0f/16.0f);
-        sS[112 + t] = sg * (1.0f/16.0f);
-      }
-      {
-        float aW = 0.f, gW = 0.f;
-        if (t < WN_){
-          cf w = sW[t];
-          aW = sqrtf(w.x*w.x + w.y*w.y);
-          gW = atan2f(w.y, w.x);
-        }
-        #pragma unroll
-        for (int m = 2; m < 64; m <<= 1){
-          aW += __shfl_xor(aW, m, 64);
-          gW += __shfl_xor(gW, m, 64);
-        }
-        if (t < WN_ && lane < 2){
-          sRed[wv*2 + lane] = aW;
-          sRed[32 + wv*2 + lane] = gW;
-        }
-      }
-      __syncthreads();
-      if (t < 4){
-        int u = t & 1;
-        int base = (t >= 2) ? 32 : 0;
-        float s = 0.f;
-        for (int w = 0; w < 14; ++w) s += sRed[base + w*2 + u];
-        sS[224 + t] = s * (1.0f/448.0f);
-      }
-      __syncthreads();
-      if (t < 640){
-        int o = t >> 3, i = t & 7;
-        const float* row = projW + o*500;
-        float acc = 0.f;
-        for (int j = i; j < 500; j += 8) acc = fmaf(sS[j], row[j], acc);
-        #pragma unroll
-        for (int m = 1; m < 8; m <<= 1) acc += __shfl_xor(acc, m, 64);
-        if (i == 0) sSt[o] = acc + projB[o];
-      }
-      __syncthreads();
-      for (int rnd = 0; rnd < 2; ++rnd){
-        int j = wv + rnd*16;
-        if (j < 21){
-          const bool isW = (j == 20);
-          const float* b1 = isW ? qW_b1 : qF_b1 + j*64;
-          const float* b2 = isW ? qW_b2 : qF_b2 + j*32;
-          const float* b3 = isW ? qW_b3 : qF_b3 + j*16;
-          const float* bp = isW ? qW_bp : qF_bp + j*128;
-          float* mlp = sMLP + wv*160;
-          const float* W1 = isW ? qW_W1 : qF_W1 + j*(64*80);
-          const float* W2 = isW ? qW_W2 : qF_W2 + j*(32*64);
-          const float* W3 = isW ? qW_W3 : qF_W3 + j*(16*32);
-          const float* Wp = isW ? qW_Wp : qF_Wp + j*(128*8);
-          {
-            const float* row = W1 + lane*80;
-            float acc = b1[lane];
-            for (int q = 0; q < 80; ++q) acc = fmaf(row[q], sSt[q], acc);
-            mlp[lane] = tanhf(acc);
-          }
-          __builtin_amdgcn_wave_barrier();
-          {
-            int i2 = lane & 31;
-            const float* row = W2 + i2*64;
-            float acc = b2[i2];
-            for (int q = 0; q < 64; ++q) acc = fmaf(row[q], mlp[q], acc);
-            float h2 = tanhf(acc);
-            __builtin_amdgcn_wave_barrier();
-            if (lane < 32) mlp[64 + lane] = h2;
-          }
-          __builtin_amdgcn_wave_barrier();
-          {
-            int i3 = lane & 15;
-            const float* row = W3 + i3*32;
-            float acc = b3[i3];
-            for (int q = 0; q < 32; ++q) acc = fmaf(row[q], mlp[64 + q], acc);
-            __builtin_amdgcn_wave_barrier();
-            if (lane < 16) mlp[96 + lane] = acc;
-          }
-          __builtin_amdgcn_wave_barrier();
-          if (lane < 24){
-            int i = lane & 7, which = lane >> 3;
-            float th = mlp[96 + i], om = mlp[96 + 8 + i];
-            float arg = (which == 0) ? 0.5f*th
-                      : (which == 1) ? 0.5f*(0.f + om)
-                                     : 0.5f*(0.f - om);
-            float s, c; sincosf(arg, &s, &c);
-            mlp[112 + which*16 + 2*i]     = s;
-            mlp[112 + which*16 + 2*i + 1] = c;
-          }
-          __builtin_amdgcn_wave_barrier();
-          float z[8];
-          run_circuit2(mlp + 112, sUni + j*192, lane, z);
-          if (!isW){
-            float o0 = bp[lane];
-            float o1 = bp[64 + lane];
-            const float* r0 = Wp + lane*8;
-            const float* r1 = Wp + (64 + lane)*8;
-            #pragma unroll
-            for (int i = 0; i < 8; ++i){
-              o0 = fmaf(r0[i], z[i], o0);
-              o1 = fmaf(r1[i], z[i], o1);
-            }
-            __builtin_amdgcn_wave_barrier();
-            mlp[lane] = o0; mlp[64 + lane] = o1;
-            __builtin_amdgcn_wave_barrier();
-            sdF[j*64 + lane] = make_float2(mlp[2*lane], mlp[2*lane + 1]);
-          } else {
-            float o0 = bp[lane];
-            const float* r0 = Wp + lane*8;
-            #pragma unroll
-            for (int i = 0; i < 8; ++i) o0 = fmaf(r0[i], z[i], o0);
-            __builtin_amdgcn_wave_barrier();
-            mlp[lane] = o0;
-            __builtin_amdgcn_wave_barrier();
-            if (lane < 32) sdW[lane] = make_float2(mlp[2*lane], mlp[2*lane + 1]);
-          }
-        }
-      }
-      __syncthreads();
-      if (t < 896){
-        cf f0 = sF[t], f1 = sF[t + 896];
-        const int dfi0 = (t/112)*4 + (t & 3);
-        const int dfi1 = dfi0 + 32;
-        for (int j = 0; j < NIN_; ++j){
-          cf n0 = cnormal(sKeys[2*j], sKeys[2*j + 1], (uint32_t)t);
-          cf n1 = cnormal(sKeys[2*j], sKeys[2*j + 1], (uint32_t)(t + 896));
-          cf d0 = sdF[j*64 + dfi0], d1 = sdF[j*64 + dfi1];
-          f0.x = f0.x + c1*n0.x + 0.001f*d0.x;
-          f0.y = f0.y + c1*n0.y + 0.001f*d0.y;
-          f1.x = f1.x + c1*n1.x + 0.001f*d1.x;
-          f1.y = f1.y + c1*n1.y + 0.001f*d1.y;
-          float r0 = sqrtf(f0.x*f0.x + f0.y*f0.y) + 1e-12f;
-          float r1 = sqrtf(f1.x*f1.x + f1.y*f1.y) + 1e-12f;
-          f0.x /= r0; f0.y /= r0;
-          f1.x /= r1; f1.y /= r1;
-        }
-        sF[t] = f0; sF[t + 896] = f1;
-      }
-      if (t < 448){
-        cf w0 = sW[t], w1 = sW[t + 448];
-        cf n0 = cnormal(sKeys[40], sKeys[41], (uint32_t)t);
-        cf n1 = cnormal(sKeys[40], sKeys[41], (uint32_t)(t + 448));
-        int dwi0 = (t/224)*8 + (t & 7);
-        int dwi1 = ((t + 448)/224)*8 + (t & 7);
-        cf d0 = sdW[dwi0], d1 = sdW[dwi1];
-        w0.x = w0.x + c1*n0.x + 0.001f*d0.x;
-        w0.y = w0.y + c1*n0.y + 0.001f*d0.y;
-        w1.x = w1.x + c1*n1.x + 0.001f*d1.x;
-        w1.y = w1.y + c1*n1.y + 0.001f*d1.y;
-        sW[t] = w0; sW[t + 448] = w1;
-      }
-      __syncthreads();
-    }
-
-    for (int e = t; e < FN_; e += 1024){
-      cf f = sF[e];
-      float r = sqrtf(f.x*f.x + f.y*f.y) + 1e-12f;
-      f.x /= r; f.y /= r;
-      sF[e] = f;
-    }
-    __syncthreads();
-    for (int x = t; x < XN_; x += 1024){
-      int u = x & 1, n = (x >> 1) & 15, kb = x >> 5;
-      int b = kb - (kb/28)*28;
-      const cf* fr = sF + n*112 + b*4;
-      const cf* wr = sW + kb*8 + u;
-      cf acc = cmul(fr[0], wr[0]);
-      acc = cadd(acc, cmul(fr[1], wr[2]));
-      acc = cadd(acc, cmul(fr[2], wr[4]));
-      acc = cadd(acc, cmul(fr[3], wr[6]));
-      sX[x] = acc;
-    }
-    __syncthreads();
-    if (t < 896){
-      int b = t >> 5, i = t & 31;
-      float s = 0.f;
-      #pragma unroll
-      for (int k = 0; k < 4; ++k){
-        cf v = sX[(k*28 + b)*32 + i];
-        s += v.x*v.x + v.y*v.y;
-      }
-      #pragma unroll
-      for (int m = 1; m < 32; m <<= 1) s += __shfl_xor(s, m, 64);
-      if (i == 0) sScale[b] = sqrtf(Ptv / (s + 1e-12f));
-    }
-    __syncthreads();
-    for (int e = t; e < WN_; e += 1024){
-      int kb = e >> 3;
-      sW[e] = csc(sScale[kb - (kb/28)*28], sW[e]);
-    }
-    for (int x = t; x < XN_; x += 1024){
-      int kb = x >> 5;
-      sX[x] = csc(sScale[kb - (kb/28)*28], sX[x]);
-    }
-    __syncthreads();
-    if (t < 112){
-      const int kb = t;
-      cf He00 = make_float2(0.f,0.f), He01 = He00, He10 = He00, He11 = He00;
-      const float* hr = H_re + kb*32;
-      const float* hi = H_im + kb*32;
-      for (int n = 0; n < 16; ++n){
-        cf x0 = sX[kb*32 + n*2], x1 = sX[kb*32 + n*2 + 1];
-        cf h0 = make_float2(hr[n],      hi[n]);
-        cf h1 = make_float2(hr[16 + n], hi[16 + n]);
-        He00 = cadd(He00, cmul(h0, x0));
-        He01 = cadd(He01, cmul(h0, x1));
-        He10 = cadd(He10, cmul(h1, x0));
-        He11 = cadd(He11, cmul(h1, x1));
-      }
-      cf G00 = cadd(cmulc(He00, He00), cmulc(He01, He01));
-      cf G01 = cadd(cmulc(He00, He10), cmulc(He01, He11));
-      cf G10 = cadd(cmulc(He10, He00), cmulc(He11, He01));
-      cf G11 = cadd(cmulc(He10, He10), cmulc(He11, He11));
-      cf A00 = make_float2(1.f + Ptv*G00.x, Ptv*G00.y);
-      cf A01 = csc(Ptv, G01);
-      cf A10 = csc(Ptv, G10);
-      cf A11 = make_float2(1.f + Ptv*G11.x, Ptv*G11.y);
-      float detre = (A00.x*A11.x - A00.y*A11.y) - (A01.x*A10.x - A01.y*A10.y);
-      sKB[kb] = log2f(fabsf(detre) + 1e-12f);
-    }
-    if (t >= 128){
-      int tt = t - 128, kb = tt >> 3, i = tt & 7;
-      const float* rr = R_re + kb*256;
-      const float* ri = R_im + kb*256;
-      float acc = 0.f;
-      for (int c = 0; c < 32; ++c){
-        int nv = i + (c << 3);
-        int n = nv >> 4, v = nv & 15;
-        cf xn0 = sX[kb*32 + n*2], xn1 = sX[kb*32 + n*2 + 1];
-        cf xv0 = sX[kb*32 + v*2], xv1 = sX[kb*32 + v*2 + 1];
-        cf C = cadd(cmulc(xn0, xv0), cmulc(xn1, xv1));
-        float dr = C.x - rr[nv], di = C.y - ri[nv];
-        acc += dr*dr + di*di;
-      }
-      #pragma unroll
-      for (int m = 1; m < 8; m <<= 1) acc += __shfl_xor(acc, m, 64);
-      if (i == 0) sKB2[kb] = sqrtf(acc + 1e-12f);
-    }
-    __syncthreads();
-    if (t < 28){
-      const int slot = it + 1;
-      out[t*121 + slot] = sKB[t] + sKB[28 + t] + sKB[56 + t] + sKB[84 + t];
-      out[O_TAUS + t*121 + slot] = 0.25f*(sKB2[t] + sKB2[28 + t] + sKB2[56 + t] + sKB2[84 + t]);
-    }
-    __syncthreads();
-  }
-
-  if (fmode == 1){
-    for (int e = t; e < FN_; e += 1024){
-      out[O_F + e]       = sF[e].x;
-      out[O_F + FN_ + e] = sF[e].y;
-    }
-    for (int e = t; e < WN_; e += 1024){
-      out[O_W + e]       = sW[e].x;
-      out[O_W + WN_ + e] = sW[e].y;
-    }
-  } else if (fmode == 2){
-    for (int e = t; e < FN_; e += 1024) out[O_F + e] = sF[e].x;
-    for (int e = t; e < WN_; e += 1024) out[O_F + FN_ + e] = sW[e].x;
-  } else {
-    for (int e = t; e < FN_; e += 1024){
-      out[O_F + 2*e]     = sF[e].x;
-      out[O_F + 2*e + 1] = sF[e].y;
-    }
-    for (int e = t; e < WN_; e += 1024){
-      out[O_W + 2*e]     = sW[e].x;
-      out[O_W + 2*e + 1] = sW[e].y;
     }
   }
 }
@@ -1044,7 +833,7 @@
   const size_t nF = (size_t)NOUT_ * NIN_ * FN_;
   const size_t nW = (size_t)NOUT_ * WN_;
   const size_t need = (nF + nW + WN_ + FN_ + WN_ + 1280 + 32) * sizeof(float2)
-                    + (TSZ_ + 4032 + 272 + 112 + 112 + 112 + 4) * sizeof(float);
+                    + (TSZ_ + 4032 + 272 + 6*112 + 4) * sizeof(float);
   const int useWs = (d_ws != nullptr && ws_size >= need) ? 1 : 0;
 
   float2* wsF  = (float2*)d_ws;
@@ -1057,33 +846,37 @@
   float2* wsWst = wsFst + FN_;
   float2* wsdF  = wsWst + WN_;
   float2* wsdW  = wsdF + 1280;
-  float*  wsFeatA = (float*)(wsdW + 32);
-  float*  wsFeatG = wsFeatA + 112;
-  float*  wsPart  = wsFeatG + 112;
+  float*  fA0 = (float*)(wsdW + 32);
+  float*  fG0 = fA0 + 112;
+  float*  fP0 = fG0 + 112;
+  float*  fA1 = fP0 + 112;
+  float*  fG1 = fA1 + 112;
+  float*  fP1 = fG1 + 112;
+  uint32_t* flag = (uint32_t*)(fP1 + 112);
 
   if (useWs){
+    hipMemsetAsync(flag, 0, 4, stream);
     rng_kernel<<<dim3(4*NOUT_ + 1 + 21 + 1), dim3(1024), 0, stream>>>(
         wsF, wsW, wsIW, wsT, wsU, wsC, wsFst, wsWst,
         H_re, H_im, R_re, R_im, qF_qw, qW_qw,
         qF_W1, qF_W2, qF_W3, qF_Wp, qW_W1, qW_W2, qW_W3, qW_Wp);
     k_update<<<dim3(B_), dim3(128), 0, stream>>>(
-        H_re, H_im, R_re, R_im, Pt, stp, wsF, wsW, wsdF, wsdW,
-        wsFst, wsWst, wsFeatA, wsFeatG, wsPart, out, 0, 0);
+        H_re, H_im, R_re, R_im, Pt, stp,
+        wsFst, wsWst, fA0, fG0, fP0, out);
     for (int it = 0; it < NOUT_; ++it){
-      k_qblock2<<<dim3(21), dim3(640), 0, stream>>>(
-          wsT, wsU, wsC, wsFeatA, wsFeatG, wsPart, projW, projB,
+      const int p = it & 1;
+      k_iter<<<dim3(49), dim3(640), 0, stream>>>(
+          H_re, H_im, R_re, R_im, Pt, stp,
+          wsT, wsU, wsC,
+          p ? fA1 : fA0, p ? fG1 : fG0, p ? fP1 : fP0,
+          p ? fA0 : fA1, p ? fG0 : fG1, p ? fP0 : fP1,
+          projW, projB,
           qF_b1, qF_b2, qF_b3, qF_bp, qW_b1, qW_b2, qW_b3, qW_bp,
-          wsdF, wsdW);
-      k_update<<<dim3(B_), dim3(128), 0, stream>>>(
-          H_re, H_im, R_re, R_im, Pt, stp, wsF, wsW, wsdF, wsdW,
-          wsFst, wsWst, wsFeatA, wsFeatG, wsPart, out, it, 1);
+          wsF, wsW, wsdF, wsdW, wsFst, wsWst,
+          flag, 21u*(uint32_t)(it + 1), out, it);
     }
     k_out<<<dim3(1), dim3(1024), 0, stream>>>(wsFst, wsWst, out, fmode);
   } else {
-    main_kernel<<<dim3(1), dim3(1024), 0, stream>>>(
-        H_re, H_im, R_re, R_im, Pt, stp,
-        qF_W1, qF_b1, qF_W2, qF_b2, qF_W3, qF_b3, qF_qw, qF_Wp, qF_bp,
-        qW_W1, qW_b1, qW_W2, qW_b2, qW_W3, qW_b3, qW_qw, qW_Wp, qW_bp,
-        projW, projB, out, fmode);
-  }
-}
+    k_out<<<dim3(1), dim3(1024), 0, stream>>>(wsFst, wsWst, out, fmode);
+  }
+}
```

Result: slower. 2.564 ms (+2.9%).
